# Performance work log

Hardware: AMD Instinct MI355X
Metric: run time of the kernel (lower is better)

The kernel has to match this reference:

```python
import jax, jax.numpy as jnp
import numpy as np

N_NODES = 100000
N_EDGES = 3200000
N_GRAPHS = 2000
IN_DIM = 12
HID = 48
ADME = 20
EPS = 1e-5


def setup_inputs() -> dict:
    key = jax.random.key(0)
    ks = jax.random.split(key, 24)
    x = jax.random.normal(ks[0], (N_NODES, IN_DIM), jnp.float32)
    edge_index = jax.random.randint(ks[1], (2, N_EDGES), 0, N_NODES, dtype=jnp.int64)
    batch = jnp.sort(jax.random.randint(ks[2], (N_NODES,), 0, N_GRAPHS, dtype=jnp.int64))
    adme = jax.random.normal(ks[3], (N_GRAPHS, ADME), jnp.float32)

    def lin(k, fo, fi):
        bound = 1.0 / np.sqrt(fi)
        return jax.random.uniform(k, (fo, fi), jnp.float32, -bound, bound)

    params = {
        # SAGEConv layer 0: lin_l (neighbors, with bias) and lin_r (root)
        'wl0': lin(ks[4], HID, IN_DIM), 'wr0': lin(ks[5], HID, IN_DIM),
        'bc0': jnp.zeros((HID,), jnp.float32),
        'g0': jnp.ones((HID,), jnp.float32), 'be0': jnp.zeros((HID,), jnp.float32),
        # SAGEConv layer 1
        'wl1': lin(ks[6], HID, HID), 'wr1': lin(ks[7], HID, HID),
        'bc1': jnp.zeros((HID,), jnp.float32),
        'g1': jnp.ones((HID,), jnp.float32), 'be1': jnp.zeros((HID,), jnp.float32),
        # head: Linear(116,64) -> BN -> ReLU -> Linear(64,32) -> ReLU -> Linear(32,1)
        'hw1': lin(ks[8], 64, 2 * HID + ADME), 'hb1': jnp.zeros((64,), jnp.float32),
        'hg1': jnp.ones((64,), jnp.float32), 'hbe1': jnp.zeros((64,), jnp.float32),
        'hw2': lin(ks[9], 32, 64), 'hb2': jnp.zeros((32,), jnp.float32),
        'hw3': lin(ks[10], 1, 32), 'hb3': jnp.zeros((1,), jnp.float32),
    }
    return dict(x=x, edge_index=edge_index, batch=batch, adme=adme, **params)


def _sage(x, src, dst, wl, wr, b):
    # mean-aggregate source features at destination nodes, then two linears
    msum = jax.ops.segment_sum(x[src], dst, num_segments=N_NODES)
    cnt = jax.ops.segment_sum(jnp.ones((src.shape[0],), x.dtype), dst, num_segments=N_NODES)
    agg = msum / jnp.maximum(cnt, 1.0)[:, None]
    return agg @ wl.T + x @ wr.T + b


def _bn(x, g, b):
    m = x.mean(0)
    v = x.var(0)  # biased variance (BatchNorm training-mode math)
    return g * (x - m) * jax.lax.rsqrt(v + EPS) + b


def reference(x, edge_index, batch, adme,
              wl0, wr0, bc0, g0, be0,
              wl1, wr1, bc1, g1, be1,
              hw1, hb1, hg1, hbe1, hw2, hb2, hw3, hb3):
    src, dst = edge_index[0], edge_index[1]
    # backbone (dropout is identity in eval)
    h = jax.nn.relu(_bn(_sage(x, src, dst, wl0, wr0, bc0), g0, be0))
    h = jax.nn.relu(_bn(_sage(h, src, dst, wl1, wr1, bc1), g1, be1))
    # global mean / max pools over graph ids
    s = jax.ops.segment_sum(h, batch, num_segments=N_GRAPHS)
    n = jax.ops.segment_sum(jnp.ones((h.shape[0],), h.dtype), batch, num_segments=N_GRAPHS)
    mean_p = s / jnp.maximum(n, 1.0)[:, None]
    max_p = jax.ops.segment_max(h, batch, num_segments=N_GRAPHS)
    max_p = jnp.where(n[:, None] > 0, max_p, 0.0)
    combined = jnp.concatenate([mean_p, max_p, adme], axis=-1)  # [B, 116]
    z = jax.nn.relu(_bn(combined @ hw1.T + hb1, hg1, hbe1))
    z = jax.nn.relu(z @ hw2.T + hb2)
    return (z @ hw3.T + hb3)[:, 0]
```

## Files before the change

kernel.cpp:

```cpp
#include <hip/hip_runtime.h>

#define NNODES  100000
#define NEDGES  3200000
#define NGRAPHS 2000
#define INDIM   12
#define HID     48
#define CEPS    1e-5f
#define CAP     96

#define BSHIFT   8
#define NBUCKET  ((NNODES + 255) / 256)
#define CAPB     8704
#define P1_BLOCKS 125
#define P1_EDGES (NEDGES / P1_BLOCKS)

#define SCAN_CHUNK 1024
#define NSCAN_BLOCKS ((NNODES + SCAN_CHUNK - 1) / SCAN_CHUNK)

__device__ inline void f4add(float4& a, const float4 b) {
  a.x += b.x; a.y += b.y; a.z += b.z; a.w += b.w;
}
__device__ inline float blo(unsigned u) { return __uint_as_float(u << 16); }
__device__ inline float bhi(unsigned u) { return __uint_as_float(u & 0xffff0000u); }
__device__ inline unsigned bpack(float a, float b) {
  unsigned ua = __float_as_uint(a), ub = __float_as_uint(b);
  ua = (ua + 0x7fffu + ((ua >> 16) & 1u)) >> 16;
  ub = (ub + 0x7fffu + ((ub >> 16) & 1u)) >> 16;
  return ua | (ub << 16);
}

__global__ __launch_bounds__(256) void convert_x_kernel(
    const float* __restrict__ x, uint4* __restrict__ xb) {
  int idx = blockIdx.x * blockDim.x + threadIdx.x;
  if (idx >= NNODES * INDIM / 8) return;
  const float4* p = (const float4*)(x + (size_t)idx * 8);
  float4 v0 = p[0], v1 = p[1];
  uint4 o;
  o.x = bpack(v0.x, v0.y); o.y = bpack(v0.z, v0.w);
  o.z = bpack(v1.x, v1.y); o.w = bpack(v1.z, v1.w);
  xb[idx] = o;
}

__global__ __launch_bounds__(256) void bucket_p1_kernel(
    const int* __restrict__ ei, int* __restrict__ bucket_cursor,
    unsigned int* __restrict__ bucketed) {
  __shared__ int hist[NBUCKET];
  __shared__ int lcur[NBUCKET];
  for (int b = threadIdx.x; b < NBUCKET; b += 256) hist[b] = 0;
  __syncthreads();
  const int base = blockIdx.x * P1_EDGES;
  for (int off = threadIdx.x * 4; off < P1_EDGES; off += 1024) {
    int4 d4 = *(const int4*)(ei + NEDGES + base + off);
    atomicAdd(&hist[(d4.x >> BSHIFT) % NBUCKET], 1);
    atomicAdd(&hist[(d4.y >> BSHIFT) % NBUCKET], 1);
    atomicAdd(&hist[(d4.z >> BSHIFT) % NBUCKET], 1);
    atomicAdd(&hist[(d4.w >> BSHIFT) % NBUCKET], 1);
  }
  __syncthreads();
  for (int b = threadIdx.x; b < NBUCKET; b += 256)
    lcur[b] = atomicAdd(&bucket_cursor[b], hist[b]);
  __syncthreads();
  for (int off = threadIdx.x * 4; off < P1_EDGES; off += 1024) {
    int4 s4 = *(const int4*)(ei + base + off);
    int4 d4 = *(const int4*)(ei + NEDGES + base + off);
    {
      int b0 = (d4.x >> BSHIFT) % NBUCKET; int p = atomicAdd(&lcur[b0], 1);
      if ((unsigned)p < (unsigned)CAPB)
        bucketed[(size_t)b0 * CAPB + p] = ((unsigned)(d4.x & 255) << 24) | ((unsigned)s4.x & 0xFFFFFFu);
    }
    {
      int b1 = (d4.y >> BSHIFT) % NBUCKET; int p = atomicAdd(&lcur[b1], 1);
      if ((unsigned)p < (unsigned)CAPB)
        bucketed[(size_t)b1 * CAPB + p] = ((unsigned)(d4.y & 255) << 24) | ((unsigned)s4.y & 0xFFFFFFu);
    }
    {
      int b2 = (d4.z >> BSHIFT) % NBUCKET; int p = atomicAdd(&lcur[b2], 1);
      if ((unsigned)p < (unsigned)CAPB)
        bucketed[(size_t)b2 * CAPB + p] = ((unsigned)(d4.z & 255) << 24) | ((unsigned)s4.z & 0xFFFFFFu);
    }
    {
      int b3 = (d4.w >> BSHIFT) % NBUCKET; int p = atomicAdd(&lcur[b3], 1);
      if ((unsigned)p < (unsigned)CAPB)
        bucketed[(size_t)b3 * CAPB + p] = ((unsigned)(d4.w & 255) << 24) | ((unsigned)s4.w & 0xFFFFFFu);
    }
  }
}

__global__ __launch_bounds__(256) void fill_p2_kernel(
    const unsigned int* __restrict__ bucketed, const int* __restrict__ bucket_cursor,
    int* __restrict__ slots, int* __restrict__ cnt) {
  __shared__ int c[256];
  c[threadIdx.x] = 0;
  __syncthreads();
  int b = blockIdx.x;
  int count = bucket_cursor[b];
  if (count > CAPB) count = CAPB;
  size_t bb = (size_t)b * CAPB;
  for (int i = threadIdx.x; i < count; i += 256) {
    unsigned v = bucketed[bb + i];
    int dl = (int)(v >> 24);
    int s = (int)(v & 0xFFFFFFu);
    int node = b * 256 + dl;
    int p = atomicAdd(&c[dl], 1);
    if (node < NNODES && (unsigned)p < (unsigned)CAP)
      slots[(size_t)node * CAP + p] = s;
  }
  __syncthreads();
  int node = b * 256 + threadIdx.x;
  if (node < NNODES) cnt[node] = min(c[threadIdx.x], CAP);
}

__global__ __launch_bounds__(256) void hist_kernel(
    const int* __restrict__ ei, int* __restrict__ cnt) {
  int t = blockIdx.x * blockDim.x + threadIdx.x;
  int e = t * 4;
  if (e >= NEDGES) return;
  int4 d4 = *(const int4*)(ei + NEDGES + e);
  atomicAdd(cnt + d4.x, 1);
  atomicAdd(cnt + d4.y, 1);
  atomicAdd(cnt + d4.z, 1);
  atomicAdd(cnt + d4.w, 1);
}

__global__ __launch_bounds__(256) void scan_bsum_kernel(
    const int* __restrict__ cnt, int* __restrict__ bsum) {
  __shared__ int s[256];
  int base = blockIdx.x * SCAN_CHUNK + threadIdx.x * 4;
  int t = 0;
#pragma unroll
  for (int k = 0; k < 4; k++) {
    int i = base + k;
    if (i < NNODES) t += cnt[i];
  }
  s[threadIdx.x] = t;
  __syncthreads();
  for (int off = 128; off; off >>= 1) {
    if (threadIdx.x < off) s[threadIdx.x] += s[threadIdx.x + off];
    __syncthreads();
  }
  if (threadIdx.x == 0) bsum[blockIdx.x] = s[0];
}

__global__ void scan_bsum_excl_kernel(int* __restrict__ bsum) {
  if (threadIdx.x == 0 && blockIdx.x == 0) {
    int acc = 0;
    for (int b = 0; b < NSCAN_BLOCKS; b++) {
      int v = bsum[b];
      bsum[b] = acc;
      acc += v;
    }
  }
}

__global__ __launch_bounds__(256) void scan_final_kernel(
    const int* __restrict__ cnt, const int* __restrict__ bsum,
    int* __restrict__ row_ptr, int* __restrict__ cursor) {
  __shared__ int s[256];
  int base = blockIdx.x * SCAN_CHUNK + threadIdx.x * 4;
  int c[4];
  int tsum = 0;
#pragma unroll
  for (int k = 0; k < 4; k++) {
    int i = base + k;
    c[k] = (i < NNODES) ? cnt[i] : 0;
    tsum += c[k];
  }
  s[threadIdx.x] = tsum;
  __syncthreads();
  for (int off = 1; off < 256; off <<= 1) {
    int x = 0;
    if (threadIdx.x >= off) x = s[threadIdx.x - off];
    __syncthreads();
    s[threadIdx.x] += x;
    __syncthreads();
  }
  int running = bsum[blockIdx.x] + s[threadIdx.x] - tsum;
#pragma unroll
  for (int k = 0; k < 4; k++) {
    int i = base + k;
    if (i < NNODES) {
      row_ptr[i] = running;
      cursor[i] = running;
      running += c[k];
    }
  }
}

__global__ __launch_bounds__(256) void fill_kernel(
    const int* __restrict__ ei, int* __restrict__ cursor,
    int* __restrict__ sorted_src) {
  int t = blockIdx.x * blockDim.x + threadIdx.x;
  int e = t * 4;
  if (e >= NEDGES) return;
  int4 s4 = *(const int4*)(ei + e);
  int4 d4 = *(const int4*)(ei + NEDGES + e);
  int p0 = atomicAdd(cursor + d4.x, 1);
  int p1 = atomicAdd(cursor + d4.y, 1);
  int p2 = atomicAdd(cursor + d4.z, 1);
  int p3 = atomicAdd(cursor + d4.w, 1);
  sorted_src[p0] = s4.x;
  sorted_src[p1] = s4.y;
  sorted_src[p2] = s4.z;
  sorted_src[p3] = s4.w;
}

__global__ __launch_bounds__(64) void graph_start_kernel(
    const int* __restrict__ batch, int* __restrict__ gstart) {
  int g = blockIdx.x * blockDim.x + threadIdx.x;
  if (g > NGRAPHS) return;
  int lo = 0, hi = NNODES;
  while (lo < hi) {
    int mid = (lo + hi) >> 1;
    if (batch[mid] < g) lo = mid + 1; else hi = mid;
  }
  gstart[g] = lo;
}

__global__ __launch_bounds__(256) void agg0_b_kernel(
    const uint2* __restrict__ xb, const int* __restrict__ slots,
    const int* __restrict__ cnt, float* __restrict__ agg) {
  int tid = blockIdx.x * blockDim.x + threadIdx.x;
  int node = tid / 3;
  int q = tid - node * 3;
  if (node >= NNODES) return;
  size_t start = (size_t)node * CAP;
  int deg = cnt[node];
  float a0[4] = {0,0,0,0}, a1[4] = {0,0,0,0}, a2[4] = {0,0,0,0}, a3[4] = {0,0,0,0};
  int n = 0;
  for (; n + 4 <= deg; n += 4) {
    int sa = slots[start + n + 0];
    int sb = slots[start + n + 1];
    int sc = slots[start + n + 2];
    int sd = slots[start + n + 3];
    uint2 ua = xb[(size_t)sa * 3 + q];
    uint2 ub = xb[(size_t)sb * 3 + q];
    uint2 uc = xb[(size_t)sc * 3 + q];
    uint2 ud = xb[(size_t)sd * 3 + q];
    a0[0] += blo(ua.x); a0[1] += bhi(ua.x); a0[2] += blo(ua.y); a0[3] += bhi(ua.y);
    a1[0] += blo(ub.x); a1[1] += bhi(ub.x); a1[2] += blo(ub.y); a1[3] += bhi(ub.y);
    a2[0] += blo(uc.x); a2[1] += bhi(uc.x); a2[2] += blo(uc.y); a2[3] += bhi(uc.y);
    a3[0] += blo(ud.x); a3[1] += bhi(ud.x); a3[2] += blo(ud.y); a3[3] += bhi(ud.y);
  }
  for (; n < deg; n++) {
    uint2 u = xb[(size_t)slots[start + n] * 3 + q];
    a0[0] += blo(u.x); a0[1] += bhi(u.x); a0[2] += blo(u.y); a0[3] += bhi(u.y);
  }
  float inv = 1.0f / fmaxf((float)deg, 1.0f);
  float4 r;
  r.x = (a0[0] + a1[0] + a2[0] + a3[0]) * inv;
  r.y = (a0[1] + a1[1] + a2[1] + a3[1]) * inv;
  r.z = (a0[2] + a1[2] + a2[2] + a3[2]) * inv;
  r.w = (a0[3] + a1[3] + a2[3] + a3[3]) * inv;
  *(float4*)(agg + (size_t)node * INDIM + q * 4) = r;
}

__global__ __launch_bounds__(256) void sage0_4k_kernel(
    const float* __restrict__ x, const float* __restrict__ agg,
    const float* __restrict__ wl, const float* __restrict__ wr,
    const float* __restrict__ bc, float* __restrict__ hpre) {
  __shared__ float swl[HID * INDIM], swr[HID * INDIM], sbc[HID];
  for (int t = threadIdx.x; t < HID * INDIM; t += 256) { swl[t] = wl[t]; swr[t] = wr[t]; }
  if (threadIdx.x < HID) sbc[threadIdx.x] = bc[threadIdx.x];
  __syncthreads();
  int tid = blockIdx.x * 256 + threadIdx.x;
  int node = tid >> 2;
  int kq = tid & 3;
  if (node >= NNODES) return;
  float xi[INDIM], ag[INDIM];
  {
    const float4* xp = (const float4*)(x + (size_t)node * INDIM);
    const float4* mp = (const float4*)(agg + (size_t)node * INDIM);
#pragma unroll
    for (int q = 0; q < 3; q++) {
      float4 v = xp[q];
      xi[q * 4 + 0] = v.x; xi[q * 4 + 1] = v.y; xi[q * 4 + 2] = v.z; xi[q * 4 + 3] = v.w;
      float4 m = mp[q];
      ag[q * 4 + 0] = m.x; ag[q * 4 + 1] = m.y; ag[q * 4 + 2] = m.z; ag[q * 4 + 3] = m.w;
    }
  }
  float o[12];
#pragma unroll
  for (int t = 0; t < 12; t++) {
    int k = kq * 12 + t;
    const float* wlr = swl + k * INDIM;
    const float* wrr = swr + k * INDIM;
    float s = sbc[k];
#pragma unroll
    for (int j = 0; j < INDIM; j++) s += ag[j] * wlr[j] + xi[j] * wrr[j];
    o[t] = s;
  }
  float* dst = hpre + (size_t)node * HID + kq * 12;
  *(float4*)(dst + 0) = make_float4(o[0], o[1], o[2], o[3]);
  *(float4*)(dst + 4) = make_float4(o[4], o[5], o[6], o[7]);
  *(float4*)(dst + 8) = make_float4(o[8], o[9], o[10], o[11]);
}

__global__ __launch_bounds__(192) void stats_kernel(
    const float* __restrict__ h, float* __restrict__ stats) {
  __shared__ float ssum[HID], ssq[HID];
  if (threadIdx.x < HID) { ssum[threadIdx.x] = 0.f; ssq[threadIdx.x] = 0.f; }
  __syncthreads();
  const int TOT = NNODES * 12;
  int base = blockIdx.x * 3072;
  float s0 = 0, s1 = 0, s2 = 0, s3 = 0, q0 = 0, q1 = 0, q2 = 0, q3 = 0;
  for (int it = 0; it < 16; ++it) {
    int idx = base + it * 192 + threadIdx.x;
    if (idx < TOT) {
      float4 v = ((const float4*)h)[idx];
      s0 += v.x; q0 += v.x * v.x;
      s1 += v.y; q1 += v.y * v.y;
      s2 += v.z; q2 += v.z * v.z;
      s3 += v.w; q3 += v.w * v.w;
    }
  }
  int kb = (threadIdx.x % 12) * 4;
  atomicAdd(&ssum[kb + 0], s0); atomicAdd(&ssq[kb + 0], q0);
  atomicAdd(&ssum[kb + 1], s1); atomicAdd(&ssq[kb + 1], q1);
  atomicAdd(&ssum[kb + 2], s2); atomicAdd(&ssq[kb + 2], q2);
  atomicAdd(&ssum[kb + 3], s3); atomicAdd(&ssq[kb + 3], q3);
  __syncthreads();
  if (threadIdx.x < HID) {
    atomicAdd(&stats[threadIdx.x], ssum[threadIdx.x]);
    atomicAdd(&stats[HID + threadIdx.x], ssq[threadIdx.x]);
  }
}

__global__ __launch_bounds__(256) void bn_relu_b16_kernel(
    const float* __restrict__ hpre, const float* __restrict__ stats,
    const float* __restrict__ g, const float* __restrict__ be,
    uint4* __restrict__ h0b) {
  __shared__ float sc[HID], sh[HID];
  if (threadIdx.x < HID) {
    int k = threadIdx.x;
    float m = stats[k] * (1.0f / NNODES);
    float v = stats[HID + k] * (1.0f / NNODES) - m * m;
    float s = g[k] * rsqrtf(v + CEPS);
    sc[k] = s; sh[k] = be[k] - m * s;
  }
  __syncthreads();
  int idx = blockIdx.x * 256 + threadIdx.x;
  if (idx >= NNODES * 6) return;
  const float4* p = (const float4*)(hpre + (size_t)idx * 8);
  float4 v0 = p[0], v1 = p[1];
  int kb = (idx % 6) * 8;
  float r0 = fmaxf(v0.x * sc[kb + 0] + sh[kb + 0], 0.f);
  float r1 = fmaxf(v0.y * sc[kb + 1] + sh[kb + 1], 0.f);
  float r2 = fmaxf(v0.z * sc[kb + 2] + sh[kb + 2], 0.f);
  float r3 = fmaxf(v0.w * sc[kb + 3] + sh[kb + 3], 0.f);
  float r4 = fmaxf(v1.x * sc[kb + 4] + sh[kb + 4], 0.f);
  float r5 = fmaxf(v1.y * sc[kb + 5] + sh[kb + 5], 0.f);
  float r6 = fmaxf(v1.z * sc[kb + 6] + sh[kb + 6], 0.f);
  float r7 = fmaxf(v1.w * sc[kb + 7] + sh[kb + 7], 0.f);
  uint4 o;
  o.x = bpack(r0, r1); o.y = bpack(r2, r3); o.z = bpack(r4, r5); o.w = bpack(r6, r7);
  h0b[idx] = o;
}

__global__ __launch_bounds__(256) void agg1_b_kernel(
    const uint4* __restrict__ h0b, const int* __restrict__ slots,
    const int* __restrict__ cnt, float* __restrict__ agg) {
  int tid = blockIdx.x * blockDim.x + threadIdx.x;
  int node = tid / 6;
  int q = tid - node * 6;
  if (node >= NNODES) return;
  size_t start = (size_t)node * CAP;
  int deg = cnt[node];
  float a0[8] = {0,0,0,0,0,0,0,0}, a1[8] = {0,0,0,0,0,0,0,0};
  float a2[8] = {0,0,0,0,0,0,0,0}, a3[8] = {0,0,0,0,0,0,0,0};
  int n = 0;
  for (; n + 4 <= deg; n += 4) {
    int sa = slots[start + n + 0];
    int sb = slots[start + n + 1];
    int sc = slots[start + n + 2];
    int sd = slots[start + n + 3];
    uint4 ua = h0b[(size_t)sa * 6 + q];
    uint4 ub = h0b[(size_t)sb * 6 + q];
    uint4 uc = h0b[(size_t)sc * 6 + q];
    uint4 ud = h0b[(size_t)sd * 6 + q];
    a0[0] += blo(ua.x); a0[1] += bhi(ua.x); a0[2] += blo(ua.y); a0[3] += bhi(ua.y);
    a0[4] += blo(ua.z); a0[5] += bhi(ua.z); a0[6] += blo(ua.w); a0[7] += bhi(ua.w);
    a1[0] += blo(ub.x); a1[1] += bhi(ub.x); a1[2] += blo(ub.y); a1[3] += bhi(ub.y);
    a1[4] += blo(ub.z); a1[5] += bhi(ub.z); a1[6] += blo(ub.w); a1[7] += bhi(ub.w);
    a2[0] += blo(uc.x); a2[1] += bhi(uc.x); a2[2] += blo(uc.y); a2[3] += bhi(uc.y);
    a2[4] += blo(uc.z); a2[5] += bhi(uc.z); a2[6] += blo(uc.w); a2[7] += bhi(uc.w);
    a3[0] += blo(ud.x); a3[1] += bhi(ud.x); a3[2] += blo(ud.y); a3[3] += bhi(ud.y);
    a3[4] += blo(ud.z); a3[5] += bhi(ud.z); a3[6] += blo(ud.w); a3[7] += bhi(ud.w);
  }
  for (; n < deg; n++) {
    uint4 u = h0b[(size_t)slots[start + n] * 6 + q];
    a0[0] += blo(u.x); a0[1] += bhi(u.x); a0[2] += blo(u.y); a0[3] += bhi(u.y);
    a0[4] += blo(u.z); a0[5] += bhi(u.z); a0[6] += blo(u.w); a0[7] += bhi(u.w);
  }
  float inv = 1.0f / fmaxf((float)deg, 1.0f);
  float* dst = agg + (size_t)node * HID + q * 8;
  float4 r0, r1;
  r0.x = (a0[0] + a1[0] + a2[0] + a3[0]) * inv;
  r0.y = (a0[1] + a1[1] + a2[1] + a3[1]) * inv;
  r0.z = (a0[2] + a1[2] + a2[2] + a3[2]) * inv;
  r0.w = (a0[3] + a1[3] + a2[3] + a3[3]) * inv;
  r1.x = (a0[4] + a1[4] + a2[4] + a3[4]) * inv;
  r1.y = (a0[5] + a1[5] + a2[5] + a3[5]) * inv;
  r1.z = (a0[6] + a1[6] + a2[6] + a3[6]) * inv;
  r1.w = (a0[7] + a1[7] + a2[7] + a3[7]) * inv;
  *(float4*)(dst + 0) = r0;
  *(float4*)(dst + 4) = r1;
}

__global__ __launch_bounds__(256) void sage1_2n_kernel(
    const float* __restrict__ agg, const uint2* __restrict__ h0b,
    const float* __restrict__ wl, const float* __restrict__ wr,
    const float* __restrict__ bc, float* __restrict__ hout) {
  __shared__ float swl[HID * HID], swr[HID * HID], sbc[HID];
  for (int t = threadIdx.x; t < HID * HID; t += 256) { swl[t] = wl[t]; swr[t] = wr[t]; }
  if (threadIdx.x < HID) sbc[threadIdx.x] = bc[threadIdx.x];
  __syncthreads();
  int tid = blockIdx.x * 256 + threadIdx.x;
  int p = tid >> 2;
  int jq = tid & 3;
  if (p >= NNODES / 2) return;
  int node0 = 2 * p, node1 = 2 * p + 1;
  const int jb = jq * 12;
  float a0[12], a1[12], h0v[12], h1v[12];
  {
    const float4* ap0 = (const float4*)(agg + (size_t)node0 * HID + jb);
    const float4* ap1 = (const float4*)(agg + (size_t)node1 * HID + jb);
#pragma unroll
    for (int q = 0; q < 3; q++) {
      float4 v = ap0[q];
      a0[q * 4 + 0] = v.x; a0[q * 4 + 1] = v.y; a0[q * 4 + 2] = v.z; a0[q * 4 + 3] = v.w;
      float4 w = ap1[q];
      a1[q * 4 + 0] = w.x; a1[q * 4 + 1] = w.y; a1[q * 4 + 2] = w.z; a1[q * 4 + 3] = w.w;
    }
    const uint2* hp0 = h0b + (size_t)node0 * 12 + jq * 3;
    const uint2* hp1 = h0b + (size_t)node1 * 12 + jq * 3;
#pragma unroll
    for (int q = 0; q < 3; q++) {
      uint2 u = hp0[q];
      h0v[q * 4 + 0] = blo(u.x); h0v[q * 4 + 1] = bhi(u.x);
      h0v[q * 4 + 2] = blo(u.y); h0v[q * 4 + 3] = bhi(u.y);
      uint2 w = hp1[q];
      h1v[q * 4 + 0] = blo(w.x); h1v[q * 4 + 1] = bhi(w.x);
      h1v[q * 4 + 2] = blo(w.y); h1v[q * 4 + 3] = bhi(w.y);
    }
  }
  float o0[12], o1[12];
#pragma unroll
  for (int k = 0; k < HID; k++) {
    const float* wlr = swl + k * HID + jb;
    const float* wrr = swr + k * HID + jb;
    float s0 = 0.f, s1 = 0.f;
#pragma unroll
    for (int j = 0; j < 12; j++) {
      float wlv = wlr[j], wrv = wrr[j];
      s0 += a0[j] * wlv + h0v[j] * wrv;
      s1 += a1[j] * wlv + h1v[j] * wrv;
    }
    s0 += __shfl_xor(s0, 1); s0 += __shfl_xor(s0, 2);
    s1 += __shfl_xor(s1, 1); s1 += __shfl_xor(s1, 2);
    if (jq == (k / 12)) {
      o0[k % 12] = s0 + sbc[k];
      o1[k % 12] = s1 + sbc[k];
    }
  }
  float* d0 = hout + (size_t)node0 * HID + jb;
  float* d1 = hout + (size_t)node1 * HID + jb;
  *(float4*)(d0 + 0) = make_float4(o0[0], o0[1], o0[2], o0[3]);
  *(float4*)(d0 + 4) = make_float4(o0[4], o0[5], o0[6], o0[7]);
  *(float4*)(d0 + 8) = make_float4(o0[8], o0[9], o0[10], o0[11]);
  *(float4*)(d1 + 0) = make_float4(o1[0], o1[1], o1[2], o1[3]);
  *(float4*)(d1 + 4) = make_float4(o1[4], o1[5], o1[6], o1[7]);
  *(float4*)(d1 + 8) = make_float4(o1[8], o1[9], o1[10], o1[11]);
}

__global__ __launch_bounds__(64) void bn_pool_kernel(
    const float* __restrict__ hpre, const float* __restrict__ stats,
    const float* __restrict__ g, const float* __restrict__ be,
    const int* __restrict__ gstart,
    float* __restrict__ meanp, float* __restrict__ maxp) {
  int gr = blockIdx.x;
  int f = threadIdx.x;
  if (f >= HID) return;
  float m = stats[f] * (1.0f / NNODES);
  float v = stats[HID + f] * (1.0f / NNODES) - m * m;
  float sc = g[f] * rsqrtf(v + CEPS);
  float sh = be[f] - m * sc;
  int start = gstart[gr], end = gstart[gr + 1];
  float sum = 0.f, mx = 0.f;
  for (int i = start; i < end; i++) {
    float val = fmaxf(hpre[(size_t)i * HID + f] * sc + sh, 0.f);
    sum += val;
    mx = fmaxf(mx, val);
  }
  float n = (float)(end - start);
  meanp[(size_t)gr * HID + f] = sum / fmaxf(n, 1.0f);
  maxp[(size_t)gr * HID + f] = mx;
}

template<bool PAD>
__global__ __launch_bounds__(256) void agg0_kernel(
    const float* __restrict__ x, const int* __restrict__ slots,
    const int* __restrict__ row_ptr, const int* __restrict__ cnt,
    float* __restrict__ agg) {
  int tid = blockIdx.x * blockDim.x + threadIdx.x;
  int node = tid / 3;
  int q = tid - node * 3;
  if (node >= NNODES) return;
  int start = PAD ? node * CAP : row_ptr[node];
  int deg = cnt[node];
  float4 a0 = {0,0,0,0}, a1 = {0,0,0,0}, a2 = {0,0,0,0}, a3 = {0,0,0,0};
  int n = 0;
  for (; n + 4 <= deg; n += 4) {
    int sa = slots[start + n + 0];
    int sb = slots[start + n + 1];
    int sc = slots[start + n + 2];
    int sd = slots[start + n + 3];
    f4add(a0, *(const float4*)(x + (size_t)sa * INDIM + q * 4));
    f4add(a1, *(const float4*)(x + (size_t)sb * INDIM + q * 4));
    f4add(a2, *(const float4*)(x + (size_t)sc * INDIM + q * 4));
    f4add(a3, *(const float4*)(x + (size_t)sd * INDIM + q * 4));
  }
  for (; n < deg; n++)
    f4add(a0, *(const float4*)(x + (size_t)slots[start + n] * INDIM + q * 4));
  f4add(a0, a1); f4add(a2, a3); f4add(a0, a2);
  float inv = 1.0f / fmaxf((float)deg, 1.0f);
  float4 r; r.x = a0.x * inv; r.y = a0.y * inv; r.z = a0.z * inv; r.w = a0.w * inv;
  *(float4*)(agg + (size_t)node * INDIM + q * 4) = r;
}

template<bool PAD>
__global__ __launch_bounds__(256) void agg1_kernel(
    const float* __restrict__ h0, const int* __restrict__ slots,
    const int* __restrict__ row_ptr, const int* __restrict__ cnt,
    float* __restrict__ agg) {
  int tid = blockIdx.x * blockDim.x + threadIdx.x;
  int node = tid / 12;
  int q = tid - node * 12;
  if (node >= NNODES) return;
  int start = PAD ? node * CAP : row_ptr[node];
  int deg = cnt[node];
  float4 a0 = {0,0,0,0}, a1 = {0,0,0,0}, a2 = {0,0,0,0}, a3 = {0,0,0,0};
  int n = 0;
  for (; n + 4 <= deg; n += 4) {
    int sa = slots[start + n + 0];
    int sb = slots[start + n + 1];
    int sc = slots[start + n + 2];
    int sd = slots[start + n + 3];
    f4add(a0, *(const float4*)(h0 + (size_t)sa * HID + q * 4));
    f4add(a1, *(const float4*)(h0 + (size_t)sb * HID + q * 4));
    f4add(a2, *(const float4*)(h0 + (size_t)sc * HID + q * 4));
    f4add(a3, *(const float4*)(h0 + (size_t)sd * HID + q * 4));
  }
  for (; n < deg; n++)
    f4add(a0, *(const float4*)(h0 + (size_t)slots[start + n] * HID + q * 4));
  f4add(a0, a1); f4add(a2, a3); f4add(a0, a2);
  float inv = 1.0f / fmaxf((float)deg, 1.0f);
  float4 r; r.x = a0.x * inv; r.y = a0.y * inv; r.z = a0.z * inv; r.w = a0.w * inv;
  *(float4*)(agg + (size_t)node * HID + q * 4) = r;
}

__global__ __launch_bounds__(256) void sage0_kernel(
    const float* __restrict__ x, const float* __restrict__ agg,
    const float* __restrict__ wl, const float* __restrict__ wr,
    const float* __restrict__ bc,
    float* __restrict__ hpre, float* __restrict__ stats) {
  __shared__ float swl[HID * INDIM], swr[HID * INDIM], sbc[HID];
  __shared__ float ssum[HID], ssq[HID];
  for (int t = threadIdx.x; t < HID * INDIM; t += blockDim.x) { swl[t] = wl[t]; swr[t] = wr[t]; }
  if (threadIdx.x < HID) { sbc[threadIdx.x] = bc[threadIdx.x]; ssum[threadIdx.x] = 0.f; ssq[threadIdx.x] = 0.f; }
  __syncthreads();
  int i = blockIdx.x * blockDim.x + threadIdx.x;
  bool valid = (i < NNODES);
  float xi[INDIM], ag[INDIM];
  if (valid) {
    const float4* xp = (const float4*)(x + (size_t)i * INDIM);
    const float4* mp = (const float4*)(agg + (size_t)i * INDIM);
#pragma unroll
    for (int q = 0; q < 3; q++) {
      float4 v = xp[q];
      xi[q * 4 + 0] = v.x; xi[q * 4 + 1] = v.y; xi[q * 4 + 2] = v.z; xi[q * 4 + 3] = v.w;
      float4 m = mp[q];
      ag[q * 4 + 0] = m.x; ag[q * 4 + 1] = m.y; ag[q * 4 + 2] = m.z; ag[q * 4 + 3] = m.w;
    }
  } else {
#pragma unroll
    for (int j = 0; j < INDIM; j++) { xi[j] = 0.f; ag[j] = 0.f; }
  }
  int lane = threadIdx.x & 63;
  for (int kb = 0; kb < HID; kb += 4) {
    float o[4];
#pragma unroll
    for (int t = 0; t < 4; t++) {
      int k = kb + t;
      float acc = valid ? sbc[k] : 0.f;
#pragma unroll
      for (int j = 0; j < INDIM; j++)
        acc += ag[j] * swl[k * INDIM + j] + xi[j] * swr[k * INDIM + j];
      o[t] = acc;
    }
    if (valid) {
      float4 v; v.x = o[0]; v.y = o[1]; v.z = o[2]; v.w = o[3];
      *((float4*)(hpre + (size_t)i * HID + kb)) = v;
    }
#pragma unroll
    for (int t = 0; t < 4; t++) {
      float s = o[t], q = o[t] * o[t];
#pragma unroll
      for (int off = 32; off; off >>= 1) { s += __shfl_xor(s, off); q += __shfl_xor(q, off); }
      if (lane == 0) { atomicAdd(&ssum[kb + t], s); atomicAdd(&ssq[kb + t], q); }
    }
  }
  __syncthreads();
  if (threadIdx.x < HID) {
    atomicAdd(&stats[threadIdx.x], ssum[threadIdx.x]);
    atomicAdd(&stats[HID + threadIdx.x], ssq[threadIdx.x]);
  }
}

__global__ __launch_bounds__(256) void bn_relu_kernel(
    float* __restrict__ h, const float* __restrict__ stats,
    const float* __restrict__ g, const float* __restrict__ be) {
  __shared__ float sc[HID], sh[HID];
  if (threadIdx.x < HID) {
    int k = threadIdx.x;
    float m = stats[k] * (1.0f / NNODES);
    float v = stats[HID + k] * (1.0f / NNODES) - m * m;
    float s = g[k] * rsqrtf(v + CEPS);
    sc[k] = s; sh[k] = be[k] - m * s;
  }
  __syncthreads();
  const int total = NNODES * (HID / 4);
  int stride = gridDim.x * blockDim.x;
  for (int idx = blockIdx.x * blockDim.x + threadIdx.x; idx < total; idx += stride) {
    int kb = (idx % (HID / 4)) * 4;
    float4 v = ((float4*)h)[idx];
    v.x = fmaxf(v.x * sc[kb + 0] + sh[kb + 0], 0.f);
    v.y = fmaxf(v.y * sc[kb + 1] + sh[kb + 1], 0.f);
    v.z = fmaxf(v.z * sc[kb + 2] + sh[kb + 2], 0.f);
    v.w = fmaxf(v.w * sc[kb + 3] + sh[kb + 3], 0.f);
    ((float4*)h)[idx] = v;
  }
}

__global__ __launch_bounds__(256) void sage1_kernel(
    const float* __restrict__ h0, float* __restrict__ agg_hpre,
    const float* __restrict__ wl, const float* __restrict__ wr,
    const float* __restrict__ bc, float* __restrict__ stats) {
  __shared__ float swl[HID * HID], swr[HID * HID], sbc[HID];
  __shared__ float ssum[HID], ssq[HID];
  for (int t = threadIdx.x; t < HID * HID; t += blockDim.x) { swl[t] = wl[t]; swr[t] = wr[t]; }
  if (threadIdx.x < HID) { sbc[threadIdx.x] = bc[threadIdx.x]; ssum[threadIdx.x] = 0.f; ssq[threadIdx.x] = 0.f; }
  __syncthreads();
  int i = blockIdx.x * blockDim.x + threadIdx.x;
  bool valid = (i < NNODES);
  float ag[HID], hx[HID];
  if (valid) {
    const float4* mp = (const float4*)(agg_hpre + (size_t)i * HID);
    const float4* hp = (const float4*)(h0 + (size_t)i * HID);
#pragma unroll
    for (int q = 0; q < HID / 4; q++) {
      float4 m = mp[q];
      ag[q * 4 + 0] = m.x; ag[q * 4 + 1] = m.y; ag[q * 4 + 2] = m.z; ag[q * 4 + 3] = m.w;
      float4 v = hp[q];
      hx[q * 4 + 0] = v.x; hx[q * 4 + 1] = v.y; hx[q * 4 + 2] = v.z; hx[q * 4 + 3] = v.w;
    }
  } else {
#pragma unroll
    for (int j = 0; j < HID; j++) { ag[j] = 0.f; hx[j] = 0.f; }
  }
  int lane = threadIdx.x & 63;
  for (int kb = 0; kb < HID; kb += 4) {
    float o[4];
#pragma unroll
    for (int t = 0; t < 4; t++) {
      int k = kb + t;
      float acc = valid ? sbc[k] : 0.f;
#pragma unroll
      for (int j = 0; j < HID; j++)
        acc += ag[j] * swl[k * HID + j] + hx[j] * swr[k * HID + j];
      o[t] = acc;
    }
    if (valid) {
      float4 v; v.x = o[0]; v.y = o[1]; v.z = o[2]; v.w = o[3];
      *((float4*)(agg_hpre + (size_t)i * HID + kb)) = v;
    }
#pragma unroll
    for (int t = 0; t < 4; t++) {
      float s = o[t], q = o[t] * o[t];
#pragma unroll
      for (int off = 32; off; off >>= 1) { s += __shfl_xor(s, off); q += __shfl_xor(q, off); }
      if (lane == 0) { atomicAdd(&ssum[kb + t], s); atomicAdd(&ssq[kb + t], q); }
    }
  }
  __syncthreads();
  if (threadIdx.x < HID) {
    atomicAdd(&stats[threadIdx.x], ssum[threadIdx.x]);
    atomicAdd(&stats[HID + threadIdx.x], ssq[threadIdx.x]);
  }
}

__global__ __launch_bounds__(64) void head1_kernel(
    const float* __restrict__ meanp, const float* __restrict__ maxp,
    const float* __restrict__ adme,
    const float* __restrict__ hw1, const float* __restrict__ hb1,
    float* __restrict__ z1) {
  int g = blockIdx.x;
  int t = threadIdx.x;
  __shared__ float comb[2 * HID + 20];
  if (t < HID) {
    comb[t] = meanp[(size_t)g * HID + t];
    comb[HID + t] = maxp[(size_t)g * HID + t];
  }
  if (t < 20) comb[2 * HID + t] = adme[(size_t)g * 20 + t];
  __syncthreads();
  float acc = hb1[t];
#pragma unroll
  for (int j = 0; j < 2 * HID + 20; j++) acc += comb[j] * hw1[t * (2 * HID + 20) + j];
  z1[(size_t)g * 64 + t] = acc;
}

__global__ __launch_bounds__(256) void headstats_kernel(
    const float* __restrict__ z1, const float* __restrict__ hg,
    const float* __restrict__ hbe, float* __restrict__ hsc, float* __restrict__ hsh) {
  int k = blockIdx.x;
  float s = 0.f, q = 0.f;
  for (int i = threadIdx.x; i < NGRAPHS; i += blockDim.x) {
    float v = z1[(size_t)i * 64 + k];
    s += v; q += v * v;
  }
  __shared__ float ls[4], lq[4];
  int lane = threadIdx.x & 63, w = threadIdx.x >> 6;
#pragma unroll
  for (int off = 32; off; off >>= 1) { s += __shfl_xor(s, off); q += __shfl_xor(q, off); }
  if (lane == 0) { ls[w] = s; lq[w] = q; }
  __syncthreads();
  if (threadIdx.x == 0) {
    s = ls[0] + ls[1] + ls[2] + ls[3];
    q = lq[0] + lq[1] + lq[2] + lq[3];
    float m = s * (1.0f / NGRAPHS);
    float v = q * (1.0f / NGRAPHS) - m * m;
    float sc = hg[k] * rsqrtf(v + CEPS);
    hsc[k] = sc; hsh[k] = hbe[k] - m * sc;
  }
}

__global__ __launch_bounds__(256) void head2_kernel(
    const float* __restrict__ z1, const float* __restrict__ hsc,
    const float* __restrict__ hsh, const float* __restrict__ hw2,
    const float* __restrict__ hb2, const float* __restrict__ hw3,
    const float* __restrict__ hb3, float* __restrict__ out) {
  __shared__ float sw2[32 * 64], sb2[32], sw3[32], ssc[64], ssh[64], sb3;
  for (int t = threadIdx.x; t < 32 * 64; t += blockDim.x) sw2[t] = hw2[t];
  if (threadIdx.x < 32) { sb2[threadIdx.x] = hb2[threadIdx.x]; sw3[threadIdx.x] = hw3[threadIdx.x]; }
  if (threadIdx.x < 64) { ssc[threadIdx.x] = hsc[threadIdx.x]; ssh[threadIdx.x] = hsh[threadIdx.x]; }
  if (threadIdx.x == 0) sb3 = hb3[0];
  __syncthreads();
  int g = blockIdx.x * blockDim.x + threadIdx.x;
  if (g >= NGRAPHS) return;
  float z[64];
#pragma unroll
  for (int k = 0; k < 64; k++) z[k] = fmaxf(z1[(size_t)g * 64 + k] * ssc[k] + ssh[k], 0.f);
  float o = sb3;
  for (int m = 0; m < 32; m++) {
    float a = sb2[m];
#pragma unroll
    for (int k = 0; k < 64; k++) a += z[k] * sw2[m * 64 + k];
    o += fmaxf(a, 0.f) * sw3[m];
  }
  out[g] = o;
}

extern "C" void kernel_launch(void* const* d_in, const int* in_sizes, int n_in,
                              void* d_out, int out_size, void* d_ws, size_t ws_size,
                              hipStream_t stream) {
  (void)in_sizes; (void)n_in; (void)out_size;
  const float* x     = (const float*)d_in[0];
  const int*   ei    = (const int*)d_in[1];
  const int*   batch = (const int*)d_in[2];
  const float* adme  = (const float*)d_in[3];
  const float* wl0 = (const float*)d_in[4];
  const float* wr0 = (const float*)d_in[5];
  const float* bc0 = (const float*)d_in[6];
  const float* g0  = (const float*)d_in[7];
  const float* be0 = (const float*)d_in[8];
  const float* wl1 = (const float*)d_in[9];
  const float* wr1 = (const float*)d_in[10];
  const float* bc1 = (const float*)d_in[11];
  const float* g1  = (const float*)d_in[12];
  const float* be1 = (const float*)d_in[13];
  const float* hw1 = (const float*)d_in[14];
  const float* hb1 = (const float*)d_in[15];
  const float* hg1 = (const float*)d_in[16];
  const float* hbe1= (const float*)d_in[17];
  const float* hw2 = (const float*)d_in[18];
  const float* hb2 = (const float*)d_in[19];
  const float* hw3 = (const float*)d_in[20];
  const float* hb3 = (const float*)d_in[21];
  float* out = (float*)d_out;

  size_t elems_A = (size_t)NNODES * HID * 2 + (size_t)NNODES * CAP + 2048
                 + 512 + NNODES + 4 * HID
                 + (size_t)NGRAPHS * HID * 2 + (size_t)NGRAPHS * 64 + 128;
  bool padded = ws_size >= elems_A * 4 + 256;

  if (padded) {
    float* buf1 = (float*)d_ws;
    float* buf2 = buf1 + (size_t)NNODES * HID;
    int* slots  = (int*)(buf2 + (size_t)NNODES * HID);
    int* gstart = slots + (size_t)NNODES * CAP;
    int* bucket_cursor = gstart + 2048;
    int* cnt    = bucket_cursor + 512;
    float* stats0 = (float*)(cnt + NNODES);
    float* stats1 = stats0 + 2 * HID;
    float* meanp = stats1 + 2 * HID;
    float* maxp  = meanp + (size_t)NGRAPHS * HID;
    float* z1  = maxp + (size_t)NGRAPHS * HID;
    float* hsc = z1 + (size_t)NGRAPHS * 64;
    float* hsh = hsc + 64;

    unsigned int* bucketed = (unsigned int*)buf2;
    uint4* h0b = (uint4*)buf1;
    uint2* xb  = (uint2*)(buf1 + 4200000);

    hipMemsetAsync(bucket_cursor, 0, 512 * sizeof(int), stream);
    hipMemsetAsync(stats0, 0, 4 * HID * sizeof(float), stream);

    convert_x_kernel<<<(NNODES * INDIM / 8 + 255) / 256, 256, 0, stream>>>(x, (uint4*)xb);
    bucket_p1_kernel<<<P1_BLOCKS, 256, 0, stream>>>(ei, bucket_cursor, bucketed);
    fill_p2_kernel<<<NBUCKET, 256, 0, stream>>>(bucketed, bucket_cursor, slots, cnt);
    graph_start_kernel<<<(NGRAPHS + 1 + 63) / 64, 64, 0, stream>>>(batch, gstart);

    agg0_b_kernel<<<(NNODES * 3 + 255) / 256, 256, 0, stream>>>(xb, slots, cnt, buf1);
    sage0_4k_kernel<<<(NNODES * 4 + 255) / 256, 256, 0, stream>>>(x, buf1, wl0, wr0, bc0, buf2);
    stats_kernel<<<(NNODES * 12 + 3071) / 3072, 192, 0, stream>>>(buf2, stats0);
    bn_relu_b16_kernel<<<(NNODES * 6 + 255) / 256, 256, 0, stream>>>(buf2, stats0, g0, be0, h0b);

    agg1_b_kernel<<<(NNODES * 6 + 255) / 256, 256, 0, stream>>>(h0b, slots, cnt, buf2);
    sage1_2n_kernel<<<(NNODES * 2 + 255) / 256, 256, 0, stream>>>(buf2, (const uint2*)h0b, wl1, wr1, bc1, buf2);
    stats_kernel<<<(NNODES * 12 + 3071) / 3072, 192, 0, stream>>>(buf2, stats1);
    bn_pool_kernel<<<NGRAPHS, 64, 0, stream>>>(buf2, stats1, g1, be1, gstart, meanp, maxp);

    head1_kernel<<<NGRAPHS, 64, 0, stream>>>(meanp, maxp, adme, hw1, hb1, z1);
    headstats_kernel<<<64, 256, 0, stream>>>(z1, hg1, hbe1, hsc, hsh);
    head2_kernel<<<(NGRAPHS + 255) / 256, 256, 0, stream>>>(z1, hsc, hsh, hw2, hb2, hw3, hb3, out);
  } else {
    float* buf1 = (float*)d_ws;
    float* buf2 = buf1 + (size_t)NNODES * HID;
    int* sorted_src = (int*)(buf2 + (size_t)NNODES * HID);
    int* row_ptr = sorted_src + NEDGES;
    int* cursor  = row_ptr + NNODES;
    int* bsum    = cursor + NNODES;
    int* gstart  = bsum + 128;
    int* cnt   = gstart + 2048;
    float* stats0 = (float*)(cnt + NNODES);
    float* stats1 = stats0 + 2 * HID;
    float* meanp = stats1 + 2 * HID;
    float* maxp  = meanp + (size_t)NGRAPHS * HID;
    float* z1  = maxp + (size_t)NGRAPHS * HID;
    float* hsc = z1 + (size_t)NGRAPHS * 64;
    float* hsh = hsc + 64;

    size_t zero_bytes = (char*)(stats1 + 2 * HID) - (char*)cnt;
    hipMemsetAsync(cnt, 0, zero_bytes, stream);

    hist_kernel<<<(NEDGES / 4 + 255) / 256, 256, 0, stream>>>(ei, cnt);
    scan_bsum_kernel<<<NSCAN_BLOCKS, 256, 0, stream>>>(cnt, bsum);
    scan_bsum_excl_kernel<<<1, 64, 0, stream>>>(bsum);
    scan_final_kernel<<<NSCAN_BLOCKS, 256, 0, stream>>>(cnt, bsum, row_ptr, cursor);
    fill_kernel<<<(NEDGES / 4 + 255) / 256, 256, 0, stream>>>(ei, cursor, sorted_src);
    graph_start_kernel<<<(NGRAPHS + 1 + 63) / 64, 64, 0, stream>>>(batch, gstart);

    agg0_kernel<false><<<(NNODES * 3 + 255) / 256, 256, 0, stream>>>(x, sorted_src, row_ptr, cnt, buf1);
    sage0_kernel<<<(NNODES + 255) / 256, 256, 0, stream>>>(x, buf1, wl0, wr0, bc0, buf2, stats0);
    bn_relu_kernel<<<2048, 256, 0, stream>>>(buf2, stats0, g0, be0);

    agg1_kernel<false><<<(NNODES * 12 + 255) / 256, 256, 0, stream>>>(buf2, sorted_src, row_ptr, cnt, buf1);
    sage1_kernel<<<(NNODES + 255) / 256, 256, 0, stream>>>(buf2, buf1, wl1, wr1, bc1, stats1);
    bn_pool_kernel<<<NGRAPHS, 64, 0, stream>>>(buf1, stats1, g1, be1, gstart, meanp, maxp);

    head1_kernel<<<NGRAPHS, 64, 0, stream>>>(meanp, maxp, adme, hw1, hb1, z1);
    headstats_kernel<<<64, 256, 0, stream>>>(z1, hg1, hbe1, hsc, hsh);
    head2_kernel<<<(NGRAPHS + 255) / 256, 256, 0, stream>>>(z1, hsc, hsh, hw2, hb2, hw3, hb3, out);
  }
}
```

Baseline: 313.7 us.

## Split neighbor slots by source half, fuse BN stats into SAGE kernels, widen pooling

Each node's neighbor slot list is now filled from both ends: sources in the lower half of the node range go at the front and the rest at the back, with the two counts packed into one int. Both aggregation kernels gather the two runs separately, which is meant to improve cache locality of the feature gathers. Batch-norm sum and sum-of-squares are now accumulated through shared-memory atomics inside the SAGE linear kernels, removing the two separate stats passes over the hidden activations. The pooling kernel moves to 256 threads with four waves splitting each graph's nodes. The cost is more shared atomics and an extra loop prologue per aggregation.

New measurement: 334.6 us. +6.7%, slower.

```diff
diff --git a/kernel.cpp b/kernel.cpp
--- a/kernel.cpp
+++ b/kernel.cpp
@@ -7,6 +7,7 @@
 #define HID     48
 #define CEPS    1e-5f
 #define CAP     96
+#define SRCMID  (NNODES / 2)
 
 #define BSHIFT   8
 #define NBUCKET  ((NNODES + 255) / 256)
@@ -89,8 +90,8 @@
 __global__ __launch_bounds__(256) void fill_p2_kernel(
     const unsigned int* __restrict__ bucketed, const int* __restrict__ bucket_cursor,
     int* __restrict__ slots, int* __restrict__ cnt) {
-  __shared__ int c[256];
-  c[threadIdx.x] = 0;
+  __shared__ int clo[256], chi[256];
+  clo[threadIdx.x] = 0; chi[threadIdx.x] = 0;
   __syncthreads();
   int b = blockIdx.x;
   int count = bucket_cursor[b];
@@ -101,13 +102,406 @@
     int dl = (int)(v >> 24);
     int s = (int)(v & 0xFFFFFFu);
     int node = b * 256 + dl;
-    int p = atomicAdd(&c[dl], 1);
-    if (node < NNODES && (unsigned)p < (unsigned)CAP)
-      slots[(size_t)node * CAP + p] = s;
+    if (node < NNODES) {
+      if (s < SRCMID) {
+        int p = atomicAdd(&clo[dl], 1);
+        if ((unsigned)p < (unsigned)CAP) slots[(size_t)node * CAP + p] = s;
+      } else {
+        int p = atomicAdd(&chi[dl], 1);
+        if ((unsigned)p < (unsigned)CAP) slots[(size_t)node * CAP + (CAP - 1 - p)] = s;
+      }
+    }
   }
   __syncthreads();
   int node = b * 256 + threadIdx.x;
-  if (node < NNODES) cnt[node] = min(c[threadIdx.x], CAP);
+  if (node < NNODES)
+    cnt[node] = min(clo[threadIdx.x], CAP) | (min(chi[threadIdx.x], CAP) << 16);
+}
+
+__global__ __launch_bounds__(64) void graph_start_kernel(
+    const int* __restrict__ batch, int* __restrict__ gstart) {
+  int g = blockIdx.x * blockDim.x + threadIdx.x;
+  if (g > NGRAPHS) return;
+  int lo = 0, hi = NNODES;
+  while (lo < hi) {
+    int mid = (lo + hi) >> 1;
+    if (batch[mid] < g) lo = mid + 1; else hi = mid;
+  }
+  gstart[g] = lo;
+}
+
+#define GATH24(BEGIN, COUNT)                                              \
+  {                                                                       \
+    int n = 0;                                                            \
+    for (; n + 4 <= (COUNT); n += 4) {                                    \
+      int sa = slots[(BEGIN) + n + 0];                                    \
+      int sb = slots[(BEGIN) + n + 1];                                    \
+      int sc = slots[(BEGIN) + n + 2];                                    \
+      int sd = slots[(BEGIN) + n + 3];                                    \
+      uint2 ua = xb[(size_t)sa * 3 + q];                                  \
+      uint2 ub = xb[(size_t)sb * 3 + q];                                  \
+      uint2 uc = xb[(size_t)sc * 3 + q];                                  \
+      uint2 ud = xb[(size_t)sd * 3 + q];                                  \
+      a0[0] += blo(ua.x); a0[1] += bhi(ua.x); a0[2] += blo(ua.y); a0[3] += bhi(ua.y); \
+      a1[0] += blo(ub.x); a1[1] += bhi(ub.x); a1[2] += blo(ub.y); a1[3] += bhi(ub.y); \
+      a2[0] += blo(uc.x); a2[1] += bhi(uc.x); a2[2] += blo(uc.y); a2[3] += bhi(uc.y); \
+      a3[0] += blo(ud.x); a3[1] += bhi(ud.x); a3[2] += blo(ud.y); a3[3] += bhi(ud.y); \
+    }                                                                     \
+    for (; n < (COUNT); n++) {                                            \
+      uint2 u = xb[(size_t)slots[(BEGIN) + n] * 3 + q];                   \
+      a0[0] += blo(u.x); a0[1] += bhi(u.x); a0[2] += blo(u.y); a0[3] += bhi(u.y); \
+    }                                                                     \
+  }
+
+__global__ __launch_bounds__(256) void agg0_b_kernel(
+    const uint2* __restrict__ xb, const int* __restrict__ slots,
+    const int* __restrict__ cnt, float* __restrict__ agg) {
+  int tid = blockIdx.x * blockDim.x + threadIdx.x;
+  int node = tid / 3;
+  int q = tid - node * 3;
+  if (node >= NNODES) return;
+  size_t start = (size_t)node * CAP;
+  int packed = cnt[node];
+  int dlo = packed & 0xFFFF, dhi = packed >> 16;
+  float a0[4] = {0,0,0,0}, a1[4] = {0,0,0,0}, a2[4] = {0,0,0,0}, a3[4] = {0,0,0,0};
+  GATH24(start, dlo);
+  GATH24(start + CAP - dhi, dhi);
+  float inv = 1.0f / fmaxf((float)(dlo + dhi), 1.0f);
+  float4 r;
+  r.x = (a0[0] + a1[0] + a2[0] + a3[0]) * inv;
+  r.y = (a0[1] + a1[1] + a2[1] + a3[1]) * inv;
+  r.z = (a0[2] + a1[2] + a2[2] + a3[2]) * inv;
+  r.w = (a0[3] + a1[3] + a2[3] + a3[3]) * inv;
+  *(float4*)(agg + (size_t)node * INDIM + q * 4) = r;
+}
+
+__global__ __launch_bounds__(256) void sage0_4k_kernel(
+    const float* __restrict__ x, const float* __restrict__ agg,
+    const float* __restrict__ wl, const float* __restrict__ wr,
+    const float* __restrict__ bc, float* __restrict__ hpre,
+    float* __restrict__ stats) {
+  __shared__ float swl[HID * INDIM], swr[HID * INDIM], sbc[HID];
+  __shared__ float ssum[HID], ssq[HID];
+  for (int t = threadIdx.x; t < HID * INDIM; t += 256) { swl[t] = wl[t]; swr[t] = wr[t]; }
+  if (threadIdx.x < HID) {
+    sbc[threadIdx.x] = bc[threadIdx.x];
+    ssum[threadIdx.x] = 0.f; ssq[threadIdx.x] = 0.f;
+  }
+  __syncthreads();
+  int tid = blockIdx.x * 256 + threadIdx.x;
+  int node = tid >> 2;
+  int kq = tid & 3;
+  bool valid = (node < NNODES);
+  float o[12];
+  if (valid) {
+    float xi[INDIM], ag[INDIM];
+    const float4* xp = (const float4*)(x + (size_t)node * INDIM);
+    const float4* mp = (const float4*)(agg + (size_t)node * INDIM);
+#pragma unroll
+    for (int q = 0; q < 3; q++) {
+      float4 v = xp[q];
+      xi[q * 4 + 0] = v.x; xi[q * 4 + 1] = v.y; xi[q * 4 + 2] = v.z; xi[q * 4 + 3] = v.w;
+      float4 m = mp[q];
+      ag[q * 4 + 0] = m.x; ag[q * 4 + 1] = m.y; ag[q * 4 + 2] = m.z; ag[q * 4 + 3] = m.w;
+    }
+#pragma unroll
+    for (int t = 0; t < 12; t++) {
+      int k = kq * 12 + t;
+      const float* wlr = swl + k * INDIM;
+      const float* wrr = swr + k * INDIM;
+      float s = sbc[k];
+#pragma unroll
+      for (int j = 0; j < INDIM; j++) s += ag[j] * wlr[j] + xi[j] * wrr[j];
+      o[t] = s;
+    }
+    float* dst = hpre + (size_t)node * HID + kq * 12;
+    *(float4*)(dst + 0) = make_float4(o[0], o[1], o[2], o[3]);
+    *(float4*)(dst + 4) = make_float4(o[4], o[5], o[6], o[7]);
+    *(float4*)(dst + 8) = make_float4(o[8], o[9], o[10], o[11]);
+#pragma unroll
+    for (int t = 0; t < 12; t++) {
+      atomicAdd(&ssum[kq * 12 + t], o[t]);
+      atomicAdd(&ssq[kq * 12 + t], o[t] * o[t]);
+    }
+  }
+  __syncthreads();
+  if (threadIdx.x < 2 * HID)
+    atomicAdd(&stats[threadIdx.x],
+              threadIdx.x < HID ? ssum[threadIdx.x] : ssq[threadIdx.x - HID]);
+}
+
+__global__ __launch_bounds__(256) void bn_relu_b16_kernel(
+    const float* __restrict__ hpre, const float* __restrict__ stats,
+    const float* __restrict__ g, const float* __restrict__ be,
+    uint4* __restrict__ h0b) {
+  __shared__ float sc[HID], sh[HID];
+  if (threadIdx.x < HID) {
+    int k = threadIdx.x;
+    float m = stats[k] * (1.0f / NNODES);
+    float v = stats[HID + k] * (1.0f / NNODES) - m * m;
+    float s = g[k] * rsqrtf(v + CEPS);
+    sc[k] = s; sh[k] = be[k] - m * s;
+  }
+  __syncthreads();
+  int idx = blockIdx.x * 256 + threadIdx.x;
+  if (idx >= NNODES * 6) return;
+  const float4* p = (const float4*)(hpre + (size_t)idx * 8);
+  float4 v0 = p[0], v1 = p[1];
+  int kb = (idx % 6) * 8;
+  float r0 = fmaxf(v0.x * sc[kb + 0] + sh[kb + 0], 0.f);
+  float r1 = fmaxf(v0.y * sc[kb + 1] + sh[kb + 1], 0.f);
+  float r2 = fmaxf(v0.z * sc[kb + 2] + sh[kb + 2], 0.f);
+  float r3 = fmaxf(v0.w * sc[kb + 3] + sh[kb + 3], 0.f);
+  float r4 = fmaxf(v1.x * sc[kb + 4] + sh[kb + 4], 0.f);
+  float r5 = fmaxf(v1.y * sc[kb + 5] + sh[kb + 5], 0.f);
+  float r6 = fmaxf(v1.z * sc[kb + 6] + sh[kb + 6], 0.f);
+  float r7 = fmaxf(v1.w * sc[kb + 7] + sh[kb + 7], 0.f);
+  uint4 o;
+  o.x = bpack(r0, r1); o.y = bpack(r2, r3); o.z = bpack(r4, r5); o.w = bpack(r6, r7);
+  h0b[idx] = o;
+}
+
+#define GATH48(BEGIN, COUNT)                                              \
+  {                                                                       \
+    int n = 0;                                                            \
+    for (; n + 4 <= (COUNT); n += 4) {                                    \
+      int sa = slots[(BEGIN) + n + 0];                                    \
+      int sb = slots[(BEGIN) + n + 1];                                    \
+      int sc = slots[(BEGIN) + n + 2];                                    \
+      int sd = slots[(BEGIN) + n + 3];                                    \
+      uint4 ua = h0b[(size_t)sa * 6 + q];                                 \
+      uint4 ub = h0b[(size_t)sb * 6 + q];                                 \
+      uint4 uc = h0b[(size_t)sc * 6 + q];                                 \
+      uint4 ud = h0b[(size_t)sd * 6 + q];                                 \
+      a0[0] += blo(ua.x); a0[1] += bhi(ua.x); a0[2] += blo(ua.y); a0[3] += bhi(ua.y); \
+      a0[4] += blo(ua.z); a0[5] += bhi(ua.z); a0[6] += blo(ua.w); a0[7] += bhi(ua.w); \
+      a1[0] += blo(ub.x); a1[1] += bhi(ub.x); a1[2] += blo(ub.y); a1[3] += bhi(ub.y); \
+      a1[4] += blo(ub.z); a1[5] += bhi(ub.z); a1[6] += blo(ub.w); a1[7] += bhi(ub.w); \
+      a2[0] += blo(uc.x); a2[1] += bhi(uc.x); a2[2] += blo(uc.y); a2[3] += bhi(uc.y); \
+      a2[4] += blo(uc.z); a2[5] += bhi(uc.z); a2[6] += blo(uc.w); a2[7] += bhi(uc.w); \
+      a3[0] += blo(ud.x); a3[1] += bhi(ud.x); a3[2] += blo(ud.y); a3[3] += bhi(ud.y); \
+      a3[4] += blo(ud.z); a3[5] += bhi(ud.z); a3[6] += blo(ud.w); a3[7] += bhi(ud.w); \
+    }                                                                     \
+    for (; n < (COUNT); n++) {                                            \
+      uint4 u = h0b[(size_t)slots[(BEGIN) + n] * 6 + q];                  \
+      a0[0] += blo(u.x); a0[1] += bhi(u.x); a0[2] += blo(u.y); a0[3] += bhi(u.y); \
+      a0[4] += blo(u.z); a0[5] += bhi(u.z); a0[6] += blo(u.w); a0[7] += bhi(u.w); \
+    }                                                                     \
+  }
+
+__global__ __launch_bounds__(256) void agg1_b_kernel(
+    const uint4* __restrict__ h0b, const int* __restrict__ slots,
+    const int* __restrict__ cnt, float* __restrict__ agg) {
+  int tid = blockIdx.x * blockDim.x + threadIdx.x;
+  int node = tid / 6;
+  int q = tid - node * 6;
+  if (node >= NNODES) return;
+  size_t start = (size_t)node * CAP;
+  int packed = cnt[node];
+  int dlo = packed & 0xFFFF, dhi = packed >> 16;
+  float a0[8] = {0,0,0,0,0,0,0,0}, a1[8] = {0,0,0,0,0,0,0,0};
+  float a2[8] = {0,0,0,0,0,0,0,0}, a3[8] = {0,0,0,0,0,0,0,0};
+  GATH48(start, dlo);
+  GATH48(start + CAP - dhi, dhi);
+  float inv = 1.0f / fmaxf((float)(dlo + dhi), 1.0f);
+  float* dst = agg + (size_t)node * HID + q * 8;
+  float4 r0, r1;
+  r0.x = (a0[0] + a1[0] + a2[0] + a3[0]) * inv;
+  r0.y = (a0[1] + a1[1] + a2[1] + a3[1]) * inv;
+  r0.z = (a0[2] + a1[2] + a2[2] + a3[2]) * inv;
+  r0.w = (a0[3] + a1[3] + a2[3] + a3[3]) * inv;
+  r1.x = (a0[4] + a1[4] + a2[4] + a3[4]) * inv;
+  r1.y = (a0[5] + a1[5] + a2[5] + a3[5]) * inv;
+  r1.z = (a0[6] + a1[6] + a2[6] + a3[6]) * inv;
+  r1.w = (a0[7] + a1[7] + a2[7] + a3[7]) * inv;
+  *(float4*)(dst + 0) = r0;
+  *(float4*)(dst + 4) = r1;
+}
+
+__global__ __launch_bounds__(256) void sage1_2n_kernel(
+    const float* __restrict__ agg, const uint2* __restrict__ h0b,
+    const float* __restrict__ wl, const float* __restrict__ wr,
+    const float* __restrict__ bc, float* __restrict__ hout,
+    float* __restrict__ stats) {
+  __shared__ float swl[HID * HID], swr[HID * HID], sbc[HID];
+  __shared__ float ssum[HID], ssq[HID];
+  for (int t = threadIdx.x; t < HID * HID; t += 256) { swl[t] = wl[t]; swr[t] = wr[t]; }
+  if (threadIdx.x < HID) {
+    sbc[threadIdx.x] = bc[threadIdx.x];
+    ssum[threadIdx.x] = 0.f; ssq[threadIdx.x] = 0.f;
+  }
+  __syncthreads();
+  int tid = blockIdx.x * 256 + threadIdx.x;
+  int p = tid >> 2;
+  int jq = tid & 3;
+  bool valid = (p < NNODES / 2);
+  const int jb = jq * 12;
+  float o0[12], o1[12];
+  int node0 = 2 * p, node1 = 2 * p + 1;
+  if (valid) {
+    float a0[12], a1[12], h0v[12], h1v[12];
+    const float4* ap0 = (const float4*)(agg + (size_t)node0 * HID + jb);
+    const float4* ap1 = (const float4*)(agg + (size_t)node1 * HID + jb);
+#pragma unroll
+    for (int q = 0; q < 3; q++) {
+      float4 v = ap0[q];
+      a0[q * 4 + 0] = v.x; a0[q * 4 + 1] = v.y; a0[q * 4 + 2] = v.z; a0[q * 4 + 3] = v.w;
+      float4 w = ap1[q];
+      a1[q * 4 + 0] = w.x; a1[q * 4 + 1] = w.y; a1[q * 4 + 2] = w.z; a1[q * 4 + 3] = w.w;
+    }
+    const uint2* hp0 = h0b + (size_t)node0 * 12 + jq * 3;
+    const uint2* hp1 = h0b + (size_t)node1 * 12 + jq * 3;
+#pragma unroll
+    for (int q = 0; q < 3; q++) {
+      uint2 u = hp0[q];
+      h0v[q * 4 + 0] = blo(u.x); h0v[q * 4 + 1] = bhi(u.x);
+      h0v[q * 4 + 2] = blo(u.y); h0v[q * 4 + 3] = bhi(u.y);
+      uint2 w = hp1[q];
+      h1v[q * 4 + 0] = blo(w.x); h1v[q * 4 + 1] = bhi(w.x);
+      h1v[q * 4 + 2] = blo(w.y); h1v[q * 4 + 3] = bhi(w.y);
+    }
+#pragma unroll
+    for (int k = 0; k < HID; k++) {
+      const float* wlr = swl + k * HID + jb;
+      const float* wrr = swr + k * HID + jb;
+      float s0 = 0.f, s1 = 0.f;
+#pragma unroll
+      for (int j = 0; j < 12; j++) {
+        float wlv = wlr[j], wrv = wrr[j];
+        s0 += a0[j] * wlv + h0v[j] * wrv;
+        s1 += a1[j] * wlv + h1v[j] * wrv;
+      }
+      s0 += __shfl_xor(s0, 1); s0 += __shfl_xor(s0, 2);
+      s1 += __shfl_xor(s1, 1); s1 += __shfl_xor(s1, 2);
+      if (jq == (k / 12)) {
+        o0[k % 12] = s0 + sbc[k];
+        o1[k % 12] = s1 + sbc[k];
+      }
+    }
+    float* d0 = hout + (size_t)node0 * HID + jb;
+    float* d1 = hout + (size_t)node1 * HID + jb;
+    *(float4*)(d0 + 0) = make_float4(o0[0], o0[1], o0[2], o0[3]);
+    *(float4*)(d0 + 4) = make_float4(o0[4], o0[5], o0[6], o0[7]);
+    *(float4*)(d0 + 8) = make_float4(o0[8], o0[9], o0[10], o0[11]);
+    *(float4*)(d1 + 0) = make_float4(o1[0], o1[1], o1[2], o1[3]);
+    *(float4*)(d1 + 4) = make_float4(o1[4], o1[5], o1[6], o1[7]);
+    *(float4*)(d1 + 8) = make_float4(o1[8], o1[9], o1[10], o1[11]);
+#pragma unroll
+    for (int t = 0; t < 12; t++) {
+      atomicAdd(&ssum[jb + t], o0[t] + o1[t]);
+      atomicAdd(&ssq[jb + t], o0[t] * o0[t] + o1[t] * o1[t]);
+    }
+  }
+  __syncthreads();
+  if (threadIdx.x < 2 * HID)
+    atomicAdd(&stats[threadIdx.x],
+              threadIdx.x < HID ? ssum[threadIdx.x] : ssq[threadIdx.x - HID]);
+}
+
+__global__ __launch_bounds__(256) void bn_pool_kernel(
+    const float* __restrict__ hpre, const float* __restrict__ stats,
+    const float* __restrict__ g, const float* __restrict__ be,
+    const int* __restrict__ gstart,
+    float* __restrict__ meanp, float* __restrict__ maxp) {
+  __shared__ float sum_s[4][HID], max_s[4][HID];
+  int gr = blockIdx.x;
+  int w = threadIdx.x >> 6;
+  int f = threadIdx.x & 63;
+  int start = gstart[gr], end = gstart[gr + 1];
+  if (f < HID) {
+    float m = stats[f] * (1.0f / NNODES);
+    float v = stats[HID + f] * (1.0f / NNODES) - m * m;
+    float sc = g[f] * rsqrtf(v + CEPS);
+    float sh = be[f] - m * sc;
+    float sum = 0.f, mx = 0.f;
+    for (int i = start + w; i < end; i += 4) {
+      float val = fmaxf(hpre[(size_t)i * HID + f] * sc + sh, 0.f);
+      sum += val;
+      mx = fmaxf(mx, val);
+    }
+    sum_s[w][f] = sum;
+    max_s[w][f] = mx;
+  }
+  __syncthreads();
+  if (threadIdx.x < HID) {
+    int k = threadIdx.x;
+    float s = sum_s[0][k] + sum_s[1][k] + sum_s[2][k] + sum_s[3][k];
+    float mx = fmaxf(fmaxf(max_s[0][k], max_s[1][k]), fmaxf(max_s[2][k], max_s[3][k]));
+    float n = (float)(end - start);
+    meanp[(size_t)gr * HID + k] = s / fmaxf(n, 1.0f);
+    maxp[(size_t)gr * HID + k] = mx;
+  }
+}
+
+__global__ __launch_bounds__(64) void head1_kernel(
+    const float* __restrict__ meanp, const float* __restrict__ maxp,
+    const float* __restrict__ adme,
+    const float* __restrict__ hw1, const float* __restrict__ hb1,
+    float* __restrict__ z1) {
+  int g = blockIdx.x;
+  int t = threadIdx.x;
+  __shared__ float comb[2 * HID + 20];
+  if (t < HID) {
+    comb[t] = meanp[(size_t)g * HID + t];
+    comb[HID + t] = maxp[(size_t)g * HID + t];
+  }
+  if (t < 20) comb[2 * HID + t] = adme[(size_t)g * 20 + t];
+  __syncthreads();
+  float acc = hb1[t];
+#pragma unroll
+  for (int j = 0; j < 2 * HID + 20; j++) acc += comb[j] * hw1[t * (2 * HID + 20) + j];
+  z1[(size_t)g * 64 + t] = acc;
+}
+
+__global__ __launch_bounds__(256) void headstats_kernel(
+    const float* __restrict__ z1, const float* __restrict__ hg,
+    const float* __restrict__ hbe, float* __restrict__ hsc, float* __restrict__ hsh) {
+  int k = blockIdx.x;
+  float s = 0.f, q = 0.f;
+  for (int i = threadIdx.x; i < NGRAPHS; i += blockDim.x) {
+    float v = z1[(size_t)i * 64 + k];
+    s += v; q += v * v;
+  }
+  __shared__ float ls[4], lq[4];
+  int lane = threadIdx.x & 63, w = threadIdx.x >> 6;
+#pragma unroll
+  for (int off = 32; off; off >>= 1) { s += __shfl_xor(s, off); q += __shfl_xor(q, off); }
+  if (lane == 0) { ls[w] = s; lq[w] = q; }
+  __syncthreads();
+  if (threadIdx.x == 0) {
+    s = ls[0] + ls[1] + ls[2] + ls[3];
+    q = lq[0] + lq[1] + lq[2] + lq[3];
+    float m = s * (1.0f / NGRAPHS);
+    float v = q * (1.0f / NGRAPHS) - m * m;
+    float sc = hg[k] * rsqrtf(v + CEPS);
+    hsc[k] = sc; hsh[k] = hbe[k] - m * sc;
+  }
+}
+
+__global__ __launch_bounds__(256) void head2_kernel(
+    const float* __restrict__ z1, const float* __restrict__ hsc,
+    const float* __restrict__ hsh, const float* __restrict__ hw2,
+    const float* __restrict__ hb2, const float* __restrict__ hw3,
+    const float* __restrict__ hb3, float* __restrict__ out) {
+  __shared__ float sw2[32 * 64], sb2[32], sw3[32], ssc[64], ssh[64], sb3;
+  for (int t = threadIdx.x; t < 32 * 64; t += blockDim.x) sw2[t] = hw2[t];
+  if (threadIdx.x < 32) { sb2[threadIdx.x] = hb2[threadIdx.x]; sw3[threadIdx.x] = hw3[threadIdx.x]; }
+  if (threadIdx.x < 64) { ssc[threadIdx.x] = hsc[threadIdx.x]; ssh[threadIdx.x] = hsh[threadIdx.x]; }
+  if (threadIdx.x == 0) sb3 = hb3[0];
+  __syncthreads();
+  int g = blockIdx.x * blockDim.x + threadIdx.x;
+  if (g >= NGRAPHS) return;
+  float z[64];
+#pragma unroll
+  for (int k = 0; k < 64; k++) z[k] = fmaxf(z1[(size_t)g * 64 + k] * ssc[k] + ssh[k], 0.f);
+  float o = sb3;
+  for (int m = 0; m < 32; m++) {
+    float a = sb2[m];
+#pragma unroll
+    for (int k = 0; k < 64; k++) a += z[k] * sw2[m * 64 + k];
+    o += fmaxf(a, 0.f) * sw3[m];
+  }
+  out[g] = o;
 }
 
 __global__ __launch_bounds__(256) void hist_kernel(
@@ -204,72 +598,58 @@
   sorted_src[p3] = s4.w;
 }
 
-__global__ __launch_bounds__(64) void graph_start_kernel(
-    const int* __restrict__ batch, int* __restrict__ gstart) {
-  int g = blockIdx.x * blockDim.x + threadIdx.x;
-  if (g > NGRAPHS) return;
-  int lo = 0, hi = NNODES;
-  while (lo < hi) {
-    int mid = (lo + hi) >> 1;
-    if (batch[mid] < g) lo = mid + 1; else hi = mid;
-  }
-  gstart[g] = lo;
-}
-
-__global__ __launch_bounds__(256) void agg0_b_kernel(
-    const uint2* __restrict__ xb, const int* __restrict__ slots,
-    const int* __restrict__ cnt, float* __restrict__ agg) {
+__global__ __launch_bounds__(256) void agg0f_kernel(
+    const float* __restrict__ x, const int* __restrict__ slots,
+    const int* __restrict__ row_ptr, const int* __restrict__ cnt,
+    float* __restrict__ agg) {
   int tid = blockIdx.x * blockDim.x + threadIdx.x;
   int node = tid / 3;
   int q = tid - node * 3;
   if (node >= NNODES) return;
-  size_t start = (size_t)node * CAP;
+  int start = row_ptr[node];
   int deg = cnt[node];
-  float a0[4] = {0,0,0,0}, a1[4] = {0,0,0,0}, a2[4] = {0,0,0,0}, a3[4] = {0,0,0,0};
-  int n = 0;
-  for (; n + 4 <= deg; n += 4) {
-    int sa = slots[start + n + 0];
-    int sb = slots[start + n + 1];
-    int sc = slots[start + n + 2];
-    int sd = slots[start + n + 3];
-    uint2 ua = xb[(size_t)sa * 3 + q];
-    uint2 ub = xb[(size_t)sb * 3 + q];
-    uint2 uc = xb[(size_t)sc * 3 + q];
-    uint2 ud = xb[(size_t)sd * 3 + q];
-    a0[0] += blo(ua.x); a0[1] += bhi(ua.x); a0[2] += blo(ua.y); a0[3] += bhi(ua.y);
-    a1[0] += blo(ub.x); a1[1] += bhi(ub.x); a1[2] += blo(ub.y); a1[3] += bhi(ub.y);
-    a2[0] += blo(uc.x); a2[1] += bhi(uc.x); a2[2] += blo(uc.y); a2[3] += bhi(uc.y);
-    a3[0] += blo(ud.x); a3[1] += bhi(ud.x); a3[2] += blo(ud.y); a3[3] += bhi(ud.y);
-  }
-  for (; n < deg; n++) {
-    uint2 u = xb[(size_t)slots[start + n] * 3 + q];
-    a0[0] += blo(u.x); a0[1] += bhi(u.x); a0[2] += blo(u.y); a0[3] += bhi(u.y);
-  }
+  float4 a0 = {0,0,0,0};
+  for (int n = 0; n < deg; n++)
+    f4add(a0, *(const float4*)(x + (size_t)slots[start + n] * INDIM + q * 4));
   float inv = 1.0f / fmaxf((float)deg, 1.0f);
-  float4 r;
-  r.x = (a0[0] + a1[0] + a2[0] + a3[0]) * inv;
-  r.y = (a0[1] + a1[1] + a2[1] + a3[1]) * inv;
-  r.z = (a0[2] + a1[2] + a2[2] + a3[2]) * inv;
-  r.w = (a0[3] + a1[3] + a2[3] + a3[3]) * inv;
+  float4 r; r.x = a0.x * inv; r.y = a0.y * inv; r.z = a0.z * inv; r.w = a0.w * inv;
   *(float4*)(agg + (size_t)node * INDIM + q * 4) = r;
 }
 
-__global__ __launch_bounds__(256) void sage0_4k_kernel(
+__global__ __launch_bounds__(256) void agg1f_kernel(
+    const float* __restrict__ h0, const int* __restrict__ slots,
+    const int* __restrict__ row_ptr, const int* __restrict__ cnt,
+    float* __restrict__ agg) {
+  int tid = blockIdx.x * blockDim.x + threadIdx.x;
+  int node = tid / 12;
+  int q = tid - node * 12;
+  if (node >= NNODES) return;
+  int start = row_ptr[node];
+  int deg = cnt[node];
+  float4 a0 = {0,0,0,0};
+  for (int n = 0; n < deg; n++)
+    f4add(a0, *(const float4*)(h0 + (size_t)slots[start + n] * HID + q * 4));
+  float inv = 1.0f / fmaxf((float)deg, 1.0f);
+  float4 r; r.x = a0.x * inv; r.y = a0.y * inv; r.z = a0.z * inv; r.w = a0.w * inv;
+  *(float4*)(agg + (size_t)node * HID + q * 4) = r;
+}
+
+__global__ __launch_bounds__(256) void sage0_kernel(
     const float* __restrict__ x, const float* __restrict__ agg,
     const float* __restrict__ wl, const float* __restrict__ wr,
-    const float* __restrict__ bc, float* __restrict__ hpre) {
+    const float* __restrict__ bc,
+    float* __restrict__ hpre, float* __restrict__ stats) {
   __shared__ float swl[HID * INDIM], swr[HID * INDIM], sbc[HID];
-  for (int t = threadIdx.x; t < HID * INDIM; t += 256) { swl[t] = wl[t]; swr[t] = wr[t]; }
-  if (threadIdx.x < HID) sbc[threadIdx.x] = bc[threadIdx.x];
-  __syncthreads();
-  int tid = blockIdx.x * 256 + threadIdx.x;
-  int node = tid >> 2;
-  int kq = tid & 3;
-  if (node >= NNODES) return;
+  __shared__ float ssum[HID], ssq[HID];
+  for (int t = threadIdx.x; t < HID * INDIM; t += blockDim.x) { swl[t] = wl[t]; swr[t] = wr[t]; }
+  if (threadIdx.x < HID) { sbc[threadIdx.x] = bc[threadIdx.x]; ssum[threadIdx.x] = 0.f; ssq[threadIdx.x] = 0.f; }
+  __syncthreads();
+  int i = blockIdx.x * blockDim.x + threadIdx.x;
+  bool valid = (i < NNODES);
   float xi[INDIM], ag[INDIM];
-  {
-    const float4* xp = (const float4*)(x + (size_t)node * INDIM);
-    const float4* mp = (const float4*)(agg + (size_t)node * INDIM);
+  if (valid) {
+    const float4* xp = (const float4*)(x + (size_t)i * INDIM);
+    const float4* mp = (const float4*)(agg + (size_t)i * INDIM);
 #pragma unroll
     for (int q = 0; q < 3; q++) {
       float4 v = xp[q];
@@ -277,47 +657,34 @@
       float4 m = mp[q];
       ag[q * 4 + 0] = m.x; ag[q * 4 + 1] = m.y; ag[q * 4 + 2] = m.z; ag[q * 4 + 3] = m.w;
     }
-  }
-  float o[12];
-#pragma unroll
-  for (int t = 0; t < 12; t++) {
-    int k = kq * 12 + t;
-    const float* wlr = swl + k * INDIM;
-    const float* wrr = swr + k * INDIM;
-    float s = sbc[k];
-#pragma unroll
-    for (int j = 0; j < INDIM; j++) s += ag[j] * wlr[j] + xi[j] * wrr[j];
-    o[t] = s;
-  }
-  float* dst = hpre + (size_t)node * HID + kq * 12;
-  *(float4*)(dst + 0) = make_float4(o[0], o[1], o[2], o[3]);
-  *(float4*)(dst + 4) = make_float4(o[4], o[5], o[6], o[7]);
-  *(float4*)(dst + 8) = make_float4(o[8], o[9], o[10], o[11]);
-}
-
-__global__ __launch_bounds__(192) void stats_kernel(
-    const float* __restrict__ h, float* __restrict__ stats) {
-  __shared__ float ssum[HID], ssq[HID];
-  if (threadIdx.x < HID) { ssum[threadIdx.x] = 0.f; ssq[threadIdx.x] = 0.f; }
-  __syncthreads();
-  const int TOT = NNODES * 12;
-  int base = blockIdx.x * 3072;
-  float s0 = 0, s1 = 0, s2 = 0, s3 = 0, q0 = 0, q1 = 0, q2 = 0, q3 = 0;
-  for (int it = 0; it < 16; ++it) {
-    int idx = base + it * 192 + threadIdx.x;
-    if (idx < TOT) {
-      float4 v = ((const float4*)h)[idx];
-      s0 += v.x; q0 += v.x * v.x;
-      s1 += v.y; q1 += v.y * v.y;
-      s2 += v.z; q2 += v.z * v.z;
-      s3 += v.w; q3 += v.w * v.w;
-    }
-  }
-  int kb = (threadIdx.x % 12) * 4;
-  atomicAdd(&ssum[kb + 0], s0); atomicAdd(&ssq[kb + 0], q0);
-  atomicAdd(&ssum[kb + 1], s1); atomicAdd(&ssq[kb + 1], q1);
-  atomicAdd(&ssum[kb + 2], s2); atomicAdd(&ssq[kb + 2], q2);
-  atomicAdd(&ssum[kb + 3], s3); atomicAdd(&ssq[kb + 3], q3);
+  } else {
+#pragma unroll
+    for (int j = 0; j < INDIM; j++) { xi[j] = 0.f; ag[j] = 0.f; }
+  }
+  int lane = threadIdx.x & 63;
+  for (int kb = 0; kb < HID; kb += 4) {
+    float o[4];
+#pragma unroll
+    for (int t = 0; t < 4; t++) {
+      int k = kb + t;
+      float acc = valid ? sbc[k] : 0.f;
+#pragma unroll
+      for (int j = 0; j < INDIM; j++)
+        acc += ag[j] * swl[k * INDIM + j] + xi[j] * swr[k * INDIM + j];
+      o[t] = acc;
+    }
+    if (valid) {
+      float4 v; v.x = o[0]; v.y = o[1]; v.z = o[2]; v.w = o[3];
+      *((float4*)(hpre + (size_t)i * HID + kb)) = v;
+    }
+#pragma unroll
+    for (int t = 0; t < 4; t++) {
+      float s = o[t], q = o[t] * o[t];
+#pragma unroll
+      for (int off = 32; off; off >>= 1) { s += __shfl_xor(s, off); q += __shfl_xor(q, off); }
+      if (lane == 0) { atomicAdd(&ssum[kb + t], s); atomicAdd(&ssq[kb + t], q); }
+    }
+  }
   __syncthreads();
   if (threadIdx.x < HID) {
     atomicAdd(&stats[threadIdx.x], ssum[threadIdx.x]);
@@ -325,10 +692,9 @@
   }
 }
 
-__global__ __launch_bounds__(256) void bn_relu_b16_kernel(
-    const float* __restrict__ hpre, const float* __restrict__ stats,
-    const float* __restrict__ g, const float* __restrict__ be,
-    uint4* __restrict__ h0b) {
+__global__ __launch_bounds__(256) void bn_relu_kernel(
+    float* __restrict__ h, const float* __restrict__ stats,
+    const float* __restrict__ g, const float* __restrict__ be) {
   __shared__ float sc[HID], sh[HID];
   if (threadIdx.x < HID) {
     int k = threadIdx.x;
@@ -338,141 +704,77 @@
     sc[k] = s; sh[k] = be[k] - m * s;
   }
   __syncthreads();
-  int idx = blockIdx.x * 256 + threadIdx.x;
-  if (idx >= NNODES * 6) return;
-  const float4* p = (const float4*)(hpre + (size_t)idx * 8);
-  float4 v0 = p[0], v1 = p[1];
-  int kb = (idx % 6) * 8;
-  float r0 = fmaxf(v0.x * sc[kb + 0] + sh[kb + 0], 0.f);
-  float r1 = fmaxf(v0.y * sc[kb + 1] + sh[kb + 1], 0.f);
-  float r2 = fmaxf(v0.z * sc[kb + 2] + sh[kb + 2], 0.f);
-  float r3 = fmaxf(v0.w * sc[kb + 3] + sh[kb + 3], 0.f);
-  float r4 = fmaxf(v1.x * sc[kb + 4] + sh[kb + 4], 0.f);
-  float r5 = fmaxf(v1.y * sc[kb + 5] + sh[kb + 5], 0.f);
-  float r6 = fmaxf(v1.z * sc[kb + 6] + sh[kb + 6], 0.f);
-  float r7 = fmaxf(v1.w * sc[kb + 7] + sh[kb + 7], 0.f);
-  uint4 o;
-  o.x = bpack(r0, r1); o.y = bpack(r2, r3); o.z = bpack(r4, r5); o.w = bpack(r6, r7);
-  h0b[idx] = o;
-}
-
-__global__ __launch_bounds__(256) void agg1_b_kernel(
-    const uint4* __restrict__ h0b, const int* __restrict__ slots,
-    const int* __restrict__ cnt, float* __restrict__ agg) {
-  int tid = blockIdx.x * blockDim.x + threadIdx.x;
-  int node = tid / 6;
-  int q = tid - node * 6;
-  if (node >= NNODES) return;
-  size_t start = (size_t)node * CAP;
-  int deg = cnt[node];
-  float a0[8] = {0,0,0,0,0,0,0,0}, a1[8] = {0,0,0,0,0,0,0,0};
-  float a2[8] = {0,0,0,0,0,0,0,0}, a3[8] = {0,0,0,0,0,0,0,0};
-  int n = 0;
-  for (; n + 4 <= deg; n += 4) {
-    int sa = slots[start + n + 0];
-    int sb = slots[start + n + 1];
-    int sc = slots[start + n + 2];
-    int sd = slots[start + n + 3];
-    uint4 ua = h0b[(size_t)sa * 6 + q];
-    uint4 ub = h0b[(size_t)sb * 6 + q];
-    uint4 uc = h0b[(size_t)sc * 6 + q];
-    uint4 ud = h0b[(size_t)sd * 6 + q];
-    a0[0] += blo(ua.x); a0[1] += bhi(ua.x); a0[2] += blo(ua.y); a0[3] += bhi(ua.y);
-    a0[4] += blo(ua.z); a0[5] += bhi(ua.z); a0[6] += blo(ua.w); a0[7] += bhi(ua.w);
-    a1[0] += blo(ub.x); a1[1] += bhi(ub.x); a1[2] += blo(ub.y); a1[3] += bhi(ub.y);
-    a1[4] += blo(ub.z); a1[5] += bhi(ub.z); a1[6] += blo(ub.w); a1[7] += bhi(ub.w);
-    a2[0] += blo(uc.x); a2[1] += bhi(uc.x); a2[2] += blo(uc.y); a2[3] += bhi(uc.y);
-    a2[4] += blo(uc.z); a2[5] += bhi(uc.z); a2[6] += blo(uc.w); a2[7] += bhi(uc.w);
-    a3[0] += blo(ud.x); a3[1] += bhi(ud.x); a3[2] += blo(ud.y); a3[3] += bhi(ud.y);
-    a3[4] += blo(ud.z); a3[5] += bhi(ud.z); a3[6] += blo(ud.w); a3[7] += bhi(ud.w);
-  }
-  for (; n < deg; n++) {
-    uint4 u = h0b[(size_t)slots[start + n] * 6 + q];
-    a0[0] += blo(u.x); a0[1] += bhi(u.x); a0[2] += blo(u.y); a0[3] += bhi(u.y);
-    a0[4] += blo(u.z); a0[5] += bhi(u.z); a0[6] += blo(u.w); a0[7] += bhi(u.w);
-  }
-  float inv = 1.0f / fmaxf((float)deg, 1.0f);
-  float* dst = agg + (size_t)node * HID + q * 8;
-  float4 r0, r1;
-  r0.x = (a0[0] + a1[0] + a2[0] + a3[0]) * inv;
-  r0.y = (a0[1] + a1[1] + a2[1] + a3[1]) * inv;
-  r0.z = (a0[2] + a1[2] + a2[2] + a3[2]) * inv;
-  r0.w = (a0[3] + a1[3] + a2[3] + a3[3]) * inv;
-  r1.x = (a0[4] + a1[4] + a2[4] + a3[4]) * inv;
-  r1.y = (a0[5] + a1[5] + a2[5] + a3[5]) * inv;
-  r1.z = (a0[6] + a1[6] + a2[6] + a3[6]) * inv;
-  r1.w = (a0[7] + a1[7] + a2[7] + a3[7]) * inv;
-  *(float4*)(dst + 0) = r0;
-  *(float4*)(dst + 4) = r1;
-}
-
-__global__ __launch_bounds__(256) void sage1_2n_kernel(
-    const float* __restrict__ agg, const uint2* __restrict__ h0b,
+  const int total = NNODES * (HID / 4);
+  int stride = gridDim.x * blockDim.x;
+  for (int idx = blockIdx.x * blockDim.x + threadIdx.x; idx < total; idx += stride) {
+    int kb = (idx % (HID / 4)) * 4;
+    float4 v = ((float4*)h)[idx];
+    v.x = fmaxf(v.x * sc[kb + 0] + sh[kb + 0], 0.f);
+    v.y = fmaxf(v.y * sc[kb + 1] + sh[kb + 1], 0.f);
+    v.z = fmaxf(v.z * sc[kb + 2] + sh[kb + 2], 0.f);
+    v.w = fmaxf(v.w * sc[kb + 3] + sh[kb + 3], 0.f);
+    ((float4*)h)[idx] = v;
+  }
+}
+
+__global__ __launch_bounds__(256) void sage1_kernel(
+    const float* __restrict__ h0, float* __restrict__ agg_hpre,
     const float* __restrict__ wl, const float* __restrict__ wr,
-    const float* __restrict__ bc, float* __restrict__ hout) {
+    const float* __restrict__ bc, float* __restrict__ stats) {
   __shared__ float swl[HID * HID], swr[HID * HID], sbc[HID];
-  for (int t = threadIdx.x; t < HID * HID; t += 256) { swl[t] = wl[t]; swr[t] = wr[t]; }
-  if (threadIdx.x < HID) sbc[threadIdx.x] = bc[threadIdx.x];
-  __syncthreads();
-  int tid = blockIdx.x * 256 + threadIdx.x;
-  int p = tid >> 2;
-  int jq = tid & 3;
-  if (p >= NNODES / 2) return;
-  int node0 = 2 * p, node1 = 2 * p + 1;
-  const int jb = jq * 12;
-  float a0[12], a1[12], h0v[12], h1v[12];
-  {
-    const float4* ap0 = (const float4*)(agg + (size_t)node0 * HID + jb);
-    const float4* ap1 = (const float4*)(agg + (size_t)node1 * HID + jb);
-#pragma unroll
-    for (int q = 0; q < 3; q++) {
-      float4 v = ap0[q];
-      a0[q * 4 + 0] = v.x; a0[q * 4 + 1] = v.y; a0[q * 4 + 2] = v.z; a0[q * 4 + 3] = v.w;
-      float4 w = ap1[q];
-      a1[q * 4 + 0] = w.x; a1[q * 4 + 1] = w.y; a1[q * 4 + 2] = w.z; a1[q * 4 + 3] = w.w;
-    }
-    const uint2* hp0 = h0b + (size_t)node0 * 12 + jq * 3;
-    const uint2* hp1 = h0b + (size_t)node1 * 12 + jq * 3;
-#pragma unroll
-    for (int q = 0; q < 3; q++) {
-      uint2 u = hp0[q];
-      h0v[q * 4 + 0] = blo(u.x); h0v[q * 4 + 1] = bhi(u.x);
-      h0v[q * 4 + 2] = blo(u.y); h0v[q * 4 + 3] = bhi(u.y);
-      uint2 w = hp1[q];
-      h1v[q * 4 + 0] = blo(w.x); h1v[q * 4 + 1] = bhi(w.x);
-      h1v[q * 4 + 2] = blo(w.y); h1v[q * 4 + 3] = bhi(w.y);
-    }
-  }
-  float o0[12], o1[12];
-#pragma unroll
-  for (int k = 0; k < HID; k++) {
-    const float* wlr = swl + k * HID + jb;
-    const float* wrr = swr + k * HID + jb;
-    float s0 = 0.f, s1 = 0.f;
-#pragma unroll
-    for (int j = 0; j < 12; j++) {
-      float wlv = wlr[j], wrv = wrr[j];
-      s0 += a0[j] * wlv + h0v[j] * wrv;
-      s1 += a1[j] * wlv + h1v[j] * wrv;
-    }
-    s0 += __shfl_xor(s0, 1); s0 += __shfl_xor(s0, 2);
-    s1 += __shfl_xor(s1, 1); s1 += __shfl_xor(s1, 2);
-    if (jq == (k / 12)) {
-      o0[k % 12] = s0 + sbc[k];
-      o1[k % 12] = s1 + sbc[k];
-    }
-  }
-  float* d0 = hout + (size_t)node0 * HID + jb;
-  float* d1 = hout + (size_t)node1 * HID + jb;
-  *(float4*)(d0 + 0) = make_float4(o0[0], o0[1], o0[2], o0[3]);
-  *(float4*)(d0 + 4) = make_float4(o0[4], o0[5], o0[6], o0[7]);
-  *(float4*)(d0 + 8) = make_float4(o0[8], o0[9], o0[10], o0[11]);
-  *(float4*)(d1 + 0) = make_float4(o1[0], o1[1], o1[2], o1[3]);
-  *(float4*)(d1 + 4) = make_float4(o1[4], o1[5], o1[6], o1[7]);
-  *(float4*)(d1 + 8) = make_float4(o1[8], o1[9], o1[10], o1[11]);
-}
-
-__global__ __launch_bounds__(64) void bn_pool_kernel(
+  __shared__ float ssum[HID], ssq[HID];
+  for (int t = threadIdx.x; t < HID * HID; t += blockDim.x) { swl[t] = wl[t]; swr[t] = wr[t]; }
+  if (threadIdx.x < HID) { sbc[threadIdx.x] = bc[threadIdx.x]; ssum[threadIdx.x] = 0.f; ssq[threadIdx.x] = 0.f; }
+  __syncthreads();
+  int i = blockIdx.x * blockDim.x + threadIdx.x;
+  bool valid = (i < NNODES);
+  float ag[HID], hx[HID];
+  if (valid) {
+    const float4* mp = (const float4*)(agg_hpre + (size_t)i * HID);
+    const float4* hp = (const float4*)(h0 + (size_t)i * HID);
+#pragma unroll
+    for (int q = 0; q < HID / 4; q++) {
+      float4 m = mp[q];
+      ag[q * 4 + 0] = m.x; ag[q * 4 + 1] = m.y; ag[q * 4 + 2] = m.z; ag[q * 4 + 3] = m.w;
+      float4 v = hp[q];
+      hx[q * 4 + 0] = v.x; hx[q * 4 + 1] = v.y; hx[q * 4 + 2] = v.z; hx[q * 4 + 3] = v.w;
+    }
+  } else {
+#pragma unroll
+    for (int j = 0; j < HID; j++) { ag[j] = 0.f; hx[j] = 0.f; }
+  }
+  int lane = threadIdx.x & 63;
+  for (int kb = 0; kb < HID; kb += 4) {
+    float o[4];
+#pragma unroll
+    for (int t = 0; t < 4; t++) {
+      int k = kb + t;
+      float acc = valid ? sbc[k] : 0.f;
+#pragma unroll
+      for (int j = 0; j < HID; j++)
+        acc += ag[j] * swl[k * HID + j] + hx[j] * swr[k * HID + j];
+      o[t] = acc;
+    }
+    if (valid) {
+      float4 v; v.x = o[0]; v.y = o[1]; v.z = o[2]; v.w = o[3];
+      *((float4*)(agg_hpre + (size_t)i * HID + kb)) = v;
+    }
+#pragma unroll
+    for (int t = 0; t < 4; t++) {
+      float s = o[t], q = o[t] * o[t];
+#pragma unroll
+      for (int off = 32; off; off >>= 1) { s += __shfl_xor(s, off); q += __shfl_xor(q, off); }
+      if (lane == 0) { atomicAdd(&ssum[kb + t], s); atomicAdd(&ssq[kb + t], q); }
+    }
+  }
+  __syncthreads();
+  if (threadIdx.x < HID) {
+    atomicAdd(&stats[threadIdx.x], ssum[threadIdx.x]);
+    atomicAdd(&stats[HID + threadIdx.x], ssq[threadIdx.x]);
+  }
+}
+
+__global__ __launch_bounds__(64) void bn_pool1w_kernel(
     const float* __restrict__ hpre, const float* __restrict__ stats,
     const float* __restrict__ g, const float* __restrict__ be,
     const int* __restrict__ gstart,
@@ -494,279 +796,6 @@
   float n = (float)(end - start);
   meanp[(size_t)gr * HID + f] = sum / fmaxf(n, 1.0f);
   maxp[(size_t)gr * HID + f] = mx;
-}
-
-template<bool PAD>
-__global__ __launch_bounds__(256) void agg0_kernel(
-    const float* __restrict__ x, const int* __restrict__ slots,
-    const int* __restrict__ row_ptr, const int* __restrict__ cnt,
-    float* __restrict__ agg) {
-  int tid = blockIdx.x * blockDim.x + threadIdx.x;
-  int node = tid / 3;
-  int q = tid - node * 3;
-  if (node >= NNODES) return;
-  int start = PAD ? node * CAP : row_ptr[node];
-  int deg = cnt[node];
-  float4 a0 = {0,0,0,0}, a1 = {0,0,0,0}, a2 = {0,0,0,0}, a3 = {0,0,0,0};
-  int n = 0;
-  for (; n + 4 <= deg; n += 4) {
-    int sa = slots[start + n + 0];
-    int sb = slots[start + n + 1];
-    int sc = slots[start + n + 2];
-    int sd = slots[start + n + 3];
-    f4add(a0, *(const float4*)(x + (size_t)sa * INDIM + q * 4));
-    f4add(a1, *(const float4*)(x + (size_t)sb * INDIM + q * 4));
-    f4add(a2, *(const float4*)(x + (size_t)sc * INDIM + q * 4));
-    f4add(a3, *(const float4*)(x + (size_t)sd * INDIM + q * 4));
-  }
-  for (; n < deg; n++)
-    f4add(a0, *(const float4*)(x + (size_t)slots[start + n] * INDIM + q * 4));
-  f4add(a0, a1); f4add(a2, a3); f4add(a0, a2);
-  float inv = 1.0f / fmaxf((float)deg, 1.0f);
-  float4 r; r.x = a0.x * inv; r.y = a0.y * inv; r.z = a0.z * inv; r.w = a0.w * inv;
-  *(float4*)(agg + (size_t)node * INDIM + q * 4) = r;
-}
-
-template<bool PAD>
-__global__ __launch_bounds__(256) void agg1_kernel(
-    const float* __restrict__ h0, const int* __restrict__ slots,
-    const int* __restrict__ row_ptr, const int* __restrict__ cnt,
-    float* __restrict__ agg) {
-  int tid = blockIdx.x * blockDim.x + threadIdx.x;
-  int node = tid / 12;
-  int q = tid - node * 12;
-  if (node >= NNODES) return;
-  int start = PAD ? node * CAP : row_ptr[node];
-  int deg = cnt[node];
-  float4 a0 = {0,0,0,0}, a1 = {0,0,0,0}, a2 = {0,0,0,0}, a3 = {0,0,0,0};
-  int n = 0;
-  for (; n + 4 <= deg; n += 4) {
-    int sa = slots[start + n + 0];
-    int sb = slots[start + n + 1];
-    int sc = slots[start + n + 2];
-    int sd = slots[start + n + 3];
-    f4add(a0, *(const float4*)(h0 + (size_t)sa * HID + q * 4));
-    f4add(a1, *(const float4*)(h0 + (size_t)sb * HID + q * 4));
-    f4add(a2, *(const float4*)(h0 + (size_t)sc * HID + q * 4));
-    f4add(a3, *(const float4*)(h0 + (size_t)sd * HID + q * 4));
-  }
-  for (; n < deg; n++)
-    f4add(a0, *(const float4*)(h0 + (size_t)slots[start + n] * HID + q * 4));
-  f4add(a0, a1); f4add(a2, a3); f4add(a0, a2);
-  float inv = 1.0f / fmaxf((float)deg, 1.0f);
-  float4 r; r.x = a0.x * inv; r.y = a0.y * inv; r.z = a0.z * inv; r.w = a0.w * inv;
-  *(float4*)(agg + (size_t)node * HID + q * 4) = r;
-}
-
-__global__ __launch_bounds__(256) void sage0_kernel(
-    const float* __restrict__ x, const float* __restrict__ agg,
-    const float* __restrict__ wl, const float* __restrict__ wr,
-    const float* __restrict__ bc,
-    float* __restrict__ hpre, float* __restrict__ stats) {
-  __shared__ float swl[HID * INDIM], swr[HID * INDIM], sbc[HID];
-  __shared__ float ssum[HID], ssq[HID];
-  for (int t = threadIdx.x; t < HID * INDIM; t += blockDim.x) { swl[t] = wl[t]; swr[t] = wr[t]; }
-  if (threadIdx.x < HID) { sbc[threadIdx.x] = bc[threadIdx.x]; ssum[threadIdx.x] = 0.f; ssq[threadIdx.x] = 0.f; }
-  __syncthreads();
-  int i = blockIdx.x * blockDim.x + threadIdx.x;
-  bool valid = (i < NNODES);
-  float xi[INDIM], ag[INDIM];
-  if (valid) {
-    const float4* xp = (const float4*)(x + (size_t)i * INDIM);
-    const float4* mp = (const float4*)(agg + (size_t)i * INDIM);
-#pragma unroll
-    for (int q = 0; q < 3; q++) {
-      float4 v = xp[q];
-      xi[q * 4 + 0] = v.x; xi[q * 4 + 1] = v.y; xi[q * 4 + 2] = v.z; xi[q * 4 + 3] = v.w;
-      float4 m = mp[q];
-      ag[q * 4 + 0] = m.x; ag[q * 4 + 1] = m.y; ag[q * 4 + 2] = m.z; ag[q * 4 + 3] = m.w;
-    }
-  } else {
-#pragma unroll
-    for (int j = 0; j < INDIM; j++) { xi[j] = 0.f; ag[j] = 0.f; }
-  }
-  int lane = threadIdx.x & 63;
-  for (int kb = 0; kb < HID; kb += 4) {
-    float o[4];
-#pragma unroll
-    for (int t = 0; t < 4; t++) {
-      int k = kb + t;
-      float acc = valid ? sbc[k] : 0.f;
-#pragma unroll
-      for (int j = 0; j < INDIM; j++)
-        acc += ag[j] * swl[k * INDIM + j] + xi[j] * swr[k * INDIM + j];
-      o[t] = acc;
-    }
-    if (valid) {
-      float4 v; v.x = o[0]; v.y = o[1]; v.z = o[2]; v.w = o[3];
-      *((float4*)(hpre + (size_t)i * HID + kb)) = v;
-    }
-#pragma unroll
-    for (int t = 0; t < 4; t++) {
-      float s = o[t], q = o[t] * o[t];
-#pragma unroll
-      for (int off = 32; off; off >>= 1) { s += __shfl_xor(s, off); q += __shfl_xor(q, off); }
-      if (lane == 0) { atomicAdd(&ssum[kb + t], s); atomicAdd(&ssq[kb + t], q); }
-    }
-  }
-  __syncthreads();
-  if (threadIdx.x < HID) {
-    atomicAdd(&stats[threadIdx.x], ssum[threadIdx.x]);
-    atomicAdd(&stats[HID + threadIdx.x], ssq[threadIdx.x]);
-  }
-}
-
-__global__ __launch_bounds__(256) void bn_relu_kernel(
-    float* __restrict__ h, const float* __restrict__ stats,
-    const float* __restrict__ g, const float* __restrict__ be) {
-  __shared__ float sc[HID], sh[HID];
-  if (threadIdx.x < HID) {
-    int k = threadIdx.x;
-    float m = stats[k] * (1.0f / NNODES);
-    float v = stats[HID + k] * (1.0f / NNODES) - m * m;
-    float s = g[k] * rsqrtf(v + CEPS);
-    sc[k] = s; sh[k] = be[k] - m * s;
-  }
-  __syncthreads();
-  const int total = NNODES * (HID / 4);
-  int stride = gridDim.x * blockDim.x;
-  for (int idx = blockIdx.x * blockDim.x + threadIdx.x; idx < total; idx += stride) {
-    int kb = (idx % (HID / 4)) * 4;
-    float4 v = ((float4*)h)[idx];
-    v.x = fmaxf(v.x * sc[kb + 0] + sh[kb + 0], 0.f);
-    v.y = fmaxf(v.y * sc[kb + 1] + sh[kb + 1], 0.f);
-    v.z = fmaxf(v.z * sc[kb + 2] + sh[kb + 2], 0.f);
-    v.w = fmaxf(v.w * sc[kb + 3] + sh[kb + 3], 0.f);
-    ((float4*)h)[idx] = v;
-  }
-}
-
-__global__ __launch_bounds__(256) void sage1_kernel(
-    const float* __restrict__ h0, float* __restrict__ agg_hpre,
-    const float* __restrict__ wl, const float* __restrict__ wr,
-    const float* __restrict__ bc, float* __restrict__ stats) {
-  __shared__ float swl[HID * HID], swr[HID * HID], sbc[HID];
-  __shared__ float ssum[HID], ssq[HID];
-  for (int t = threadIdx.x; t < HID * HID; t += blockDim.x) { swl[t] = wl[t]; swr[t] = wr[t]; }
-  if (threadIdx.x < HID) { sbc[threadIdx.x] = bc[threadIdx.x]; ssum[threadIdx.x] = 0.f; ssq[threadIdx.x] = 0.f; }
-  __syncthreads();
-  int i = blockIdx.x * blockDim.x + threadIdx.x;
-  bool valid = (i < NNODES);
-  float ag[HID], hx[HID];
-  if (valid) {
-    const float4* mp = (const float4*)(agg_hpre + (size_t)i * HID);
-    const float4* hp = (const float4*)(h0 + (size_t)i * HID);
-#pragma unroll
-    for (int q = 0; q < HID / 4; q++) {
-      float4 m = mp[q];
-      ag[q * 4 + 0] = m.x; ag[q * 4 + 1] = m.y; ag[q * 4 + 2] = m.z; ag[q * 4 + 3] = m.w;
-      float4 v = hp[q];
-      hx[q * 4 + 0] = v.x; hx[q * 4 + 1] = v.y; hx[q * 4 + 2] = v.z; hx[q * 4 + 3] = v.w;
-    }
-  } else {
-#pragma unroll
-    for (int j = 0; j < HID; j++) { ag[j] = 0.f; hx[j] = 0.f; }
-  }
-  int lane = threadIdx.x & 63;
-  for (int kb = 0; kb < HID; kb += 4) {
-    float o[4];
-#pragma unroll
-    for (int t = 0; t < 4; t++) {
-      int k = kb + t;
-      float acc = valid ? sbc[k] : 0.f;
-#pragma unroll
-      for (int j = 0; j < HID; j++)
-        acc += ag[j] * swl[k * HID + j] + hx[j] * swr[k * HID + j];
-      o[t] = acc;
-    }
-    if (valid) {
-      float4 v; v.x = o[0]; v.y = o[1]; v.z = o[2]; v.w = o[3];
-      *((float4*)(agg_hpre + (size_t)i * HID + kb)) = v;
-    }
-#pragma unroll
-    for (int t = 0; t < 4; t++) {
-      float s = o[t], q = o[t] * o[t];
-#pragma unroll
-      for (int off = 32; off; off >>= 1) { s += __shfl_xor(s, off); q += __shfl_xor(q, off); }
-      if (lane == 0) { atomicAdd(&ssum[kb + t], s); atomicAdd(&ssq[kb + t], q); }
-    }
-  }
-  __syncthreads();
-  if (threadIdx.x < HID) {
-    atomicAdd(&stats[threadIdx.x], ssum[threadIdx.x]);
-    atomicAdd(&stats[HID + threadIdx.x], ssq[threadIdx.x]);
-  }
-}
-
-__global__ __launch_bounds__(64) void head1_kernel(
-    const float* __restrict__ meanp, const float* __restrict__ maxp,
-    const float* __restrict__ adme,
-    const float* __restrict__ hw1, const float* __restrict__ hb1,
-    float* __restrict__ z1) {
-  int g = blockIdx.x;
-  int t = threadIdx.x;
-  __shared__ float comb[2 * HID + 20];
-  if (t < HID) {
-    comb[t] = meanp[(size_t)g * HID + t];
-    comb[HID + t] = maxp[(size_t)g * HID + t];
-  }
-  if (t < 20) comb[2 * HID + t] = adme[(size_t)g * 20 + t];
-  __syncthreads();
-  float acc = hb1[t];
-#pragma unroll
-  for (int j = 0; j < 2 * HID + 20; j++) acc += comb[j] * hw1[t * (2 * HID + 20) + j];
-  z1[(size_t)g * 64 + t] = acc;
-}
-
-__global__ __launch_bounds__(256) void headstats_kernel(
-    const float* __restrict__ z1, const float* __restrict__ hg,
-    const float* __restrict__ hbe, float* __restrict__ hsc, float* __restrict__ hsh) {
-  int k = blockIdx.x;
-  float s = 0.f, q = 0.f;
-  for (int i = threadIdx.x; i < NGRAPHS; i += blockDim.x) {
-    float v = z1[(size_t)i * 64 + k];
-    s += v; q += v * v;
-  }
-  __shared__ float ls[4], lq[4];
-  int lane = threadIdx.x & 63, w = threadIdx.x >> 6;
-#pragma unroll
-  for (int off = 32; off; off >>= 1) { s += __shfl_xor(s, off); q += __shfl_xor(q, off); }
-  if (lane == 0) { ls[w] = s; lq[w] = q; }
-  __syncthreads();
-  if (threadIdx.x == 0) {
-    s = ls[0] + ls[1] + ls[2] + ls[3];
-    q = lq[0] + lq[1] + lq[2] + lq[3];
-    float m = s * (1.0f / NGRAPHS);
-    float v = q * (1.0f / NGRAPHS) - m * m;
-    float sc = hg[k] * rsqrtf(v + CEPS);
-    hsc[k] = sc; hsh[k] = hbe[k] - m * sc;
-  }
-}
-
-__global__ __launch_bounds__(256) void head2_kernel(
-    const float* __restrict__ z1, const float* __restrict__ hsc,
-    const float* __restrict__ hsh, const float* __restrict__ hw2,
-    const float* __restrict__ hb2, const float* __restrict__ hw3,
-    const float* __restrict__ hb3, float* __restrict__ out) {
-  __shared__ float sw2[32 * 64], sb2[32], sw3[32], ssc[64], ssh[64], sb3;
-  for (int t = threadIdx.x; t < 32 * 64; t += blockDim.x) sw2[t] = hw2[t];
-  if (threadIdx.x < 32) { sb2[threadIdx.x] = hb2[threadIdx.x]; sw3[threadIdx.x] = hw3[threadIdx.x]; }
-  if (threadIdx.x < 64) { ssc[threadIdx.x] = hsc[threadIdx.x]; ssh[threadIdx.x] = hsh[threadIdx.x]; }
-  if (threadIdx.x == 0) sb3 = hb3[0];
-  __syncthreads();
-  int g = blockIdx.x * blockDim.x + threadIdx.x;
-  if (g >= NGRAPHS) return;
-  float z[64];
-#pragma unroll
-  for (int k = 0; k < 64; k++) z[k] = fmaxf(z1[(size_t)g * 64 + k] * ssc[k] + ssh[k], 0.f);
-  float o = sb3;
-  for (int m = 0; m < 32; m++) {
-    float a = sb2[m];
-#pragma unroll
-    for (int k = 0; k < 64; k++) a += z[k] * sw2[m * 64 + k];
-    o += fmaxf(a, 0.f) * sw3[m];
-  }
-  out[g] = o;
 }
 
 extern "C" void kernel_launch(void* const* d_in, const int* in_sizes, int n_in,
@@ -830,14 +859,12 @@
     graph_start_kernel<<<(NGRAPHS + 1 + 63) / 64, 64, 0, stream>>>(batch, gstart);
 
     agg0_b_kernel<<<(NNODES * 3 + 255) / 256, 256, 0, stream>>>(xb, slots, cnt, buf1);
-    sage0_4k_kernel<<<(NNODES * 4 + 255) / 256, 256, 0, stream>>>(x, buf1, wl0, wr0, bc0, buf2);
-    stats_kernel<<<(NNODES * 12 + 3071) / 3072, 192, 0, stream>>>(buf2, stats0);
+    sage0_4k_kernel<<<(NNODES * 4 + 255) / 256, 256, 0, stream>>>(x, buf1, wl0, wr0, bc0, buf2, stats0);
     bn_relu_b16_kernel<<<(NNODES * 6 + 255) / 256, 256, 0, stream>>>(buf2, stats0, g0, be0, h0b);
 
     agg1_b_kernel<<<(NNODES * 6 + 255) / 256, 256, 0, stream>>>(h0b, slots, cnt, buf2);
-    sage1_2n_kernel<<<(NNODES * 2 + 255) / 256, 256, 0, stream>>>(buf2, (const uint2*)h0b, wl1, wr1, bc1, buf2);
-    stats_kernel<<<(NNODES * 12 + 3071) / 3072, 192, 0, stream>>>(buf2, stats1);
-    bn_pool_kernel<<<NGRAPHS, 64, 0, stream>>>(buf2, stats1, g1, be1, gstart, meanp, maxp);
+    sage1_2n_kernel<<<(NNODES * 2 + 255) / 256, 256, 0, stream>>>(buf2, (const uint2*)h0b, wl1, wr1, bc1, buf2, stats1);
+    bn_pool_kernel<<<NGRAPHS, 256, 0, stream>>>(buf2, stats1, g1, be1, gstart, meanp, maxp);
 
     head1_kernel<<<NGRAPHS, 64, 0, stream>>>(meanp, maxp, adme, hw1, hb1, z1);
     headstats_kernel<<<64, 256, 0, stream>>>(z1, hg1, hbe1, hsc, hsh);
@@ -869,13 +896,13 @@
     fill_kernel<<<(NEDGES / 4 + 255) / 256, 256, 0, stream>>>(ei, cursor, sorted_src);
     graph_start_kernel<<<(NGRAPHS + 1 + 63) / 64, 64, 0, stream>>>(batch, gstart);
 
-    agg0_kernel<false><<<(NNODES * 3 + 255) / 256, 256, 0, stream>>>(x, sorted_src, row_ptr, cnt, buf1);
+    agg0f_kernel<<<(NNODES * 3 + 255) / 256, 256, 0, stream>>>(x, sorted_src, row_ptr, cnt, buf1);
     sage0_kernel<<<(NNODES + 255) / 256, 256, 0, stream>>>(x, buf1, wl0, wr0, bc0, buf2, stats0);
     bn_relu_kernel<<<2048, 256, 0, stream>>>(buf2, stats0, g0, be0);
 
-    agg1_kernel<false><<<(NNODES * 12 + 255) / 256, 256, 0, stream>>>(buf2, sorted_src, row_ptr, cnt, buf1);
+    agg1f_kernel<<<(NNODES * 12 + 255) / 256, 256, 0, stream>>>(buf2, sorted_src, row_ptr, cnt, buf1);
     sage1_kernel<<<(NNODES + 255) / 256, 256, 0, stream>>>(buf2, buf1, wl1, wr1, bc1, stats1);
-    bn_pool_kernel<<<NGRAPHS, 64, 0, stream>>>(buf1, stats1, g1, be1, gstart, meanp, maxp);
+    bn_pool1w_kernel<<<NGRAPHS, 64, 0, stream>>>(buf1, stats1, g1, be1, gstart, meanp, maxp);
 
     head1_kernel<<<NGRAPHS, 64, 0, stream>>>(meanp, maxp, adme, hw1, hb1, z1);
     headstats_kernel<<<64, 256, 0, stream>>>(z1, hg1, hbe1, hsc, hsh);
```
